# Optimization experiments

Hardware: AMD Instinct MI355X
Metric: run time of the kernel (lower is better)

The kernel has to match this reference:

```python
import jax, jax.numpy as jnp
import numpy as np
from jax import lax

EPS = 1e-5
C, H, W, G = 512, 32, 32, 32


def instance_norm(x):
    # torch InstanceNorm2d: affine=False, biased variance over (H,W)
    mu = x.mean(axis=(2, 3), keepdims=True)
    var = ((x - mu) ** 2).mean(axis=(2, 3), keepdims=True)
    return (x - mu) / jnp.sqrt(var + EPS)


def conv2d(x, w, stride=1, padding=0, groups=1, lhs_dilation=None):
    return lax.conv_general_dilated(
        x, w, (stride, stride), [(padding, padding)] * 2,
        lhs_dilation=lhs_dilation, feature_group_count=groups,
        dimension_numbers=('NCHW', 'OIHW', 'NCHW'))


def leaky_relu(x):
    return jnp.where(x >= 0, x, 0.2 * x)


def unfold(img, k, s):
    # img: (C,H,W) -> (nH*nW, C, k, k); matches torch unfold(1,k,s).unfold(2,k,s)
    c, h, w = img.shape
    nH = (h - k) // s + 1
    nW = (w - k) // s + 1
    rows = []
    for i in range(k):
        cols = [img[:, i:i + s * (nH - 1) + 1:s, j:j + s * (nW - 1) + 1:s] for j in range(k)]
        rows.append(jnp.stack(cols, axis=-1))  # (C,nH,nW,k)
    p = jnp.stack(rows, axis=-2)  # (C,nH,nW,k,k)
    return p.transpose(1, 2, 0, 3, 4).reshape(nH * nW, c, k, k)


def ral(bg, fg, rate=2, ksize=3, scale=10.0):
    # Region Affinity Layer (contextual-attention style), batch = 1
    b, c, h, w = fg.shape
    fh, fw = h // rate, w // rate
    # bilinear downsample by exactly 2 (half-pixel) == 2x2 average pooling
    fg_small = fg.reshape(b, c, fh, rate, fw, rate).mean(axis=(3, 5))
    bk = 2 * rate
    bg_patches = unfold(jnp.pad(bg, ((0, 0), (0, 0), (1, 1), (1, 1)))[0], bk, rate)      # (256,C,4,4)
    fg_patches = unfold(jnp.pad(fg_small, ((0, 0), (0, 0), (1, 1), (1, 1)))[0], ksize, 1)  # (256,C,3,3)
    norm = jnp.sqrt((fg_patches ** 2).sum(axis=(1, 2, 3), keepdims=True))
    fgp_n = fg_patches / jnp.maximum(norm, 1e-4)
    score = conv2d(fg_small, fgp_n, padding=1)        # (1,256,16,16)
    attn = jax.nn.softmax(score * scale, axis=1)
    # conv_transpose2d(attn, bg_patches, stride=rate, padding=1) via lhs dilation
    w_t = jnp.flip(bg_patches, axis=(-2, -1)).transpose(1, 0, 2, 3)  # (C,256,4,4)
    return conv2d(attn, w_t, padding=bk - 2, lhs_dilation=(rate, rate)) / 4.0  # (1,C,32,32)


def forward(x, gus, w_sk3, b_sk3, w_sk5, b_sk5, w_sk7, b_sk7,
            w_fc, b_fc, w_fc0, b_fc0, w_fc1, b_fc1, w_fc2, b_fc2, w_down, w_fuse):
    # ---- SKConv (M=3 branches: k=3/5/7, groups=32) ----
    feas = []
    for wgt, bias, pad in ((w_sk3, b_sk3, 1), (w_sk5, b_sk5, 2), (w_sk7, b_sk7, 3)):
        f = conv2d(x, wgt, padding=pad, groups=G) + bias[None, :, None, None]
        feas.append(jax.nn.relu(instance_norm(f)))
    feas = jnp.stack(feas, axis=1)                # (B,3,C,H,W)
    fea_s = feas.sum(axis=1).mean(axis=(2, 3))    # (B,C) global pool
    fea_z = fea_s @ w_fc.T + b_fc                 # (B,32)
    att = jnp.stack([fea_z @ w_fc0.T + b_fc0,
                     fea_z @ w_fc1.T + b_fc1,
                     fea_z @ w_fc2.T + b_fc2], axis=1)  # (B,3,C)
    att = jax.nn.softmax(att, axis=1)[..., None, None]
    out_32 = (feas * att).sum(axis=1)             # (1,C,32,32)
    out_res = out_32
    out_32 = ral(out_32, out_32)
    b, c, h, w = out_32.shape
    # ---- gaussian-weighted broadcast sum: (P,H,W)x(C,H,W)->(P,C)->raw reshape ----
    gus_out = jnp.einsum('pxy,cxy->pc', gus, out_32[0]).reshape(b, c, h, w)
    # ---- CSA patch correlation ----
    csa2_in = jax.nn.sigmoid(out_32)
    p_fff = unfold(jnp.pad(out_32, ((0, 0), (0, 0), (1, 1), (1, 1)))[0], 3, 1)    # (1024,C,3,3)
    p_f = unfold(jnp.pad(csa2_in, ((0, 0), (0, 0), (1, 1), (1, 1)))[0], 3, 1)     # (1024,C,3,3)
    p_conv = unfold(csa2_in[0], 1, 1)                                             # (1024,C,1,1)
    csa_a = (p_conv * p_f).mean(axis=1)                                           # (1024,3,3)
    csa_a = jax.nn.softmax(csa_a.reshape(h * w, 9), axis=1).reshape(h * w, 1, 3, 3)
    out_csa = (csa_a * p_fff).sum(axis=(-2, -1)).reshape(b, c, h, w)
    # ---- fuse ----
    z = jnp.concatenate([gus_out, out_csa], axis=1)       # (1,1024,32,32)
    z = leaky_relu(instance_norm(conv2d(z, w_down)))
    z = jnp.concatenate([z, out_res], axis=1)             # (1,1024,32,32)
    return leaky_relu(instance_norm(conv2d(z, w_fuse)))   # (1,512,32,32)


def _gaussian_buffer():
    # util.gussin(1.5): gaussian centered at every grid position of a 32x32 map
    v = 1.5
    r = np.arange(32)
    i, k, x, y = np.meshgrid(r, r, r, r, indexing='ij')
    g = np.exp(-((x - i) ** 2 + (y - k) ** 2) / (2 * v * v)) / (2 * np.pi * v * v)
    return jnp.asarray(g.reshape(32 * 32, 32, 32), dtype=jnp.float32)


def setup_inputs():
    key = jax.random.key(0)
    ks = jax.random.split(key, 12)
    s = 0.02
    return {
        'x': jax.random.normal(ks[0], (1, C, H, W), jnp.float32),
        'gus': _gaussian_buffer(),
        'w_sk3': jax.random.normal(ks[1], (C, C // G, 3, 3), jnp.float32) * s,
        'b_sk3': jnp.zeros((C,), jnp.float32),
        'w_sk5': jax.random.normal(ks[2], (C, C // G, 5, 5), jnp.float32) * s,
        'b_sk5': jnp.zeros((C,), jnp.float32),
        'w_sk7': jax.random.normal(ks[3], (C, C // G, 7, 7), jnp.float32) * s,
        'b_sk7': jnp.zeros((C,), jnp.float32),
        'w_fc': jax.random.normal(ks[4], (32, C), jnp.float32) * s,
        'b_fc': jnp.zeros((32,), jnp.float32),
        'w_fc0': jax.random.normal(ks[5], (C, 32), jnp.float32) * s,
        'b_fc0': jnp.zeros((C,), jnp.float32),
        'w_fc1': jax.random.normal(ks[6], (C, 32), jnp.float32) * s,
        'b_fc1': jnp.zeros((C,), jnp.float32),
        'w_fc2': jax.random.normal(ks[7], (C, 32), jnp.float32) * s,
        'b_fc2': jnp.zeros((C,), jnp.float32),
        'w_down': jax.random.normal(ks[8], (512, 1024, 1, 1), jnp.float32) * s,
        'w_fuse': jax.random.normal(ks[9], (512, 1024, 1, 1), jnp.float32) * s,
    }


def reference(x, gus, w_sk3, b_sk3, w_sk5, b_sk5, w_sk7, b_sk7, w_fc, b_fc,
              w_fc0, b_fc0, w_fc1, b_fc1, w_fc2, b_fc2, w_down, w_fuse):
    return forward(x, gus, w_sk3, b_sk3, w_sk5, b_sk5, w_sk7, b_sk7,
                   w_fc, b_fc, w_fc0, b_fc0, w_fc1, b_fc1, w_fc2, b_fc2,
                   w_down, w_fuse)
```

## Files before the change

### kernel.cpp

```cpp
#include <hip/hip_runtime.h>
#include <math.h>

#define EPSN 1e-5f

typedef __attribute__((ext_vector_type(8))) short bf16x8;
typedef __attribute__((ext_vector_type(4))) float f32x4;

__device__ __forceinline__ ushort f2bf(float f) {
  unsigned u = __float_as_uint(f);
  unsigned r = (u + 0x7fff + ((u >> 16) & 1)) >> 16;
  return (ushort)r;
}
__device__ __forceinline__ float bf2f(ushort h) {
  return __uint_as_float(((unsigned)h) << 16);
}

__device__ __forceinline__ void breduce2(float& a, float& b, float* lds) {
#pragma unroll
  for (int o = 32; o > 0; o >>= 1) {
    a += __shfl_down(a, o);
    b += __shfl_down(b, o);
  }
  int lane = threadIdx.x & 63, wid = threadIdx.x >> 6;
  __syncthreads();
  if (lane == 0) { lds[wid] = a; lds[4 + wid] = b; }
  __syncthreads();
  a = lds[0] + lds[1] + lds[2] + lds[3];
  b = lds[4] + lds[5] + lds[6] + lds[7];
}

__device__ __forceinline__ float breduce_sum(float v, float* lds) {
#pragma unroll
  for (int o = 32; o > 0; o >>= 1) v += __shfl_down(v, o);
  int lane = threadIdx.x & 63, wid = threadIdx.x >> 6;
  __syncthreads();
  if (lane == 0) lds[wid] = v;
  __syncthreads();
  return lds[0] + lds[1] + lds[2] + lds[3];
}

__device__ __forceinline__ float breduce_max(float v, float* lds) {
#pragma unroll
  for (int o = 32; o > 0; o >>= 1) v = fmaxf(v, __shfl_down(v, o));
  int lane = threadIdx.x & 63, wid = threadIdx.x >> 6;
  __syncthreads();
  if (lane == 0) lds[wid] = v;
  __syncthreads();
  return fmaxf(fmaxf(lds[0], lds[1]), fmaxf(lds[2], lds[3]));
}

__global__ void pre_kernel(const float* __restrict__ gus,
                           const float* __restrict__ wdown,
                           const float* __restrict__ wfuse,
                           const float* __restrict__ w3,
                           const float* __restrict__ w5,
                           const float* __restrict__ w7,
                           ushort* __restrict__ gus_bf,
                           ushort* __restrict__ wdown_bf,
                           ushort* __restrict__ wfuse_bf,
                           ushort* __restrict__ resd,
                           ushort* __restrict__ Apk_g,
                           ushort* __restrict__ Acomb,
                           float* __restrict__ diagsum) {
  int bid = blockIdx.x, tid = threadIdx.x;
  if (bid < 2048) {
    int i = bid * 1024 + tid * 4;
    if (i < 1048576) {
      float4 v = *(const float4*)&gus[i];
      int m = i >> 10, n = i & 1023;
      int y = n >> 5, x = n & 31;
      int idxb = ((y >> 1) << 4) + (x >> 1);
      int py = y & 1;
      ushort2 e0 = {f2bf(v.x), f2bf(v.z)};
      ushort2 e1 = {f2bf(v.y), f2bf(v.w)};
      *(ushort2*)&gus_bf[(size_t)m * 1024 + (py * 2 + 0) * 256 + idxb] = e0;
      *(ushort2*)&gus_bf[(size_t)m * 1024 + (py * 2 + 1) * 256 + idxb] = e1;
    } else {
      const float* src; ushort* dst; int off;
      if (i < 1572864) { src = wdown; dst = wdown_bf; off = i - 1048576; }
      else { src = wfuse; dst = wfuse_bf; off = i - 1572864; }
      float4 v = *(const float4*)&src[off];
      ushort4 o = {f2bf(v.x), f2bf(v.y), f2bf(v.z), f2bf(v.w)};
      *(ushort4*)&dst[off] = o;
    }
  } else if (bid < 2304) {
    int t8 = (bid - 2048) * 256 + tid;
    uint4 z = {0u, 0u, 0u, 0u};
#pragma unroll
    for (int k = 0; k < 4; ++k) *(uint4*)&resd[(size_t)(t8 + k * 65536) * 8] = z;
  } else if (bid < 5056) {
    int i2 = (bid - 2304) * 256 + tid;
    int g = i2 / 22016;
    int r = i2 - g * 22016;
    int p = r >> 9;
    int r5 = r & 511;
    int quad = r5 >> 7, m16 = (r5 >> 3) & 15, j = r & 7;
    int k = quad * 8 + j, tp = k >> 4, ic = k & 15;
    float val = 0.f;
    if (p < 25) {
      int t = 2 * p + tp;
      if (t < 49) val = w7[(size_t)(g * 16 + m16) * 784 + ic * 49 + t];
    } else if (p < 38) {
      int t = 2 * (p - 25) + tp;
      if (t < 25) val = w5[(size_t)(g * 16 + m16) * 400 + ic * 25 + t];
    } else {
      int t = 2 * (p - 38) + tp;
      if (t < 9) val = w3[(size_t)(g * 16 + m16) * 144 + ic * 9 + t];
    }
    Apk_g[i2] = f2bf(val);
  } else if (bid < 5568) {
    int j = (bid - 5056) * 256 + tid;
    uint4 z = {0u, 0u, 0u, 0u};
    ((uint4*)Acomb)[j] = z;
  } else {
    diagsum[tid] = 0.f;
  }
}

__global__ __launch_bounds__(256) void sk_mfma(const float* __restrict__ x,
                                               const ushort* __restrict__ Apk_g,
                                               ushort* __restrict__ feasRawH) {
  __shared__ ushort xg[10 * 38 * 24];
  int bid = blockIdx.x, tid = threadIdx.x;
  int g = bid >> 3, sl = bid & 7, y0 = sl * 4;
  for (int i = tid; i < 4560; i += 256) ((uint*)xg)[i] = 0u;
  __syncthreads();
  for (int i = tid; i < 5120; i += 256) {
    int lr = i >> 9, ic = (i >> 5) & 15, xc = i & 31;
    int y = y0 + lr - 3;
    if ((unsigned)y < 32u)
      xg[(lr * 38 + xc + 3) * 24 + ic] =
          f2bf(x[(size_t)(g * 16 + ic) * 1024 + y * 32 + xc]);
  }
  __syncthreads();
  int wv = tid >> 6, lane = tid & 63, quad = lane >> 4, m16 = lane & 15;
  int qh = (quad & 1) * 8, tp = quad >> 1;
  const ushort* Ag = Apk_g + (size_t)g * 22016;
  f32x4 acc[2][3] = {};
#pragma unroll
  for (int p = 0; p < 25; ++p) {
    bf16x8 af = *(const bf16x8*)&Ag[(p * 4 + quad) * 128 + m16 * 8];
    int t = 2 * p + tp;
    if (t > 48) t = 48;
    int ky = t / 7, kx = t - ky * 7;
#pragma unroll
    for (int ti = 0; ti < 2; ++ti) {
      int T = wv + ti * 4, tl = T >> 1, x0c = (T & 1) * 16;
      bf16x8 bf = *(const bf16x8*)&xg[((tl + ky) * 38 + x0c + m16 + kx) * 24 + qh];
      acc[ti][2] = __builtin_amdgcn_mfma_f32_16x16x32_bf16(af, bf, acc[ti][2], 0, 0, 0);
    }
  }
#pragma unroll
  for (int p = 0; p < 13; ++p) {
    bf16x8 af = *(const bf16x8*)&Ag[((p + 25) * 4 + quad) * 128 + m16 * 8];
    int t = 2 * p + tp;
    if (t > 24) t = 24;
    int ky = t / 5, kx = t - ky * 5;
#pragma unroll
    for (int ti = 0; ti < 2; ++ti) {
      int T = wv + ti * 4, tl = T >> 1, x0c = (T & 1) * 16;
      bf16x8 bf =
          *(const bf16x8*)&xg[((tl + ky + 1) * 38 + x0c + m16 + kx + 1) * 24 + qh];
      acc[ti][1] = __builtin_amdgcn_mfma_f32_16x16x32_bf16(af, bf, acc[ti][1], 0, 0, 0);
    }
  }
#pragma unroll
  for (int p = 0; p < 5; ++p) {
    bf16x8 af = *(const bf16x8*)&Ag[((p + 38) * 4 + quad) * 128 + m16 * 8];
    int t = 2 * p + tp;
    if (t > 8) t = 8;
    int ky = t / 3, kx = t - ky * 3;
#pragma unroll
    for (int ti = 0; ti < 2; ++ti) {
      int T = wv + ti * 4, tl = T >> 1, x0c = (T & 1) * 16;
      bf16x8 bf =
          *(const bf16x8*)&xg[((tl + ky + 2) * 38 + x0c + m16 + kx + 2) * 24 + qh];
      acc[ti][0] = __builtin_amdgcn_mfma_f32_16x16x32_bf16(af, bf, acc[ti][0], 0, 0, 0);
    }
  }
  int cb = g * 16 + quad * 4;
#pragma unroll
  for (int ti = 0; ti < 2; ++ti) {
    int T = wv + ti * 4, tl = T >> 1, x0c = (T & 1) * 16;
    int pos = (y0 + tl) * 32 + x0c + m16;
#pragma unroll
    for (int br = 0; br < 3; ++br)
#pragma unroll
      for (int r = 0; r < 4; ++r)
        feasRawH[(size_t)(br * 512 + cb + r) * 1024 + pos] = f2bf(acc[ti][br][r]);
  }
}

__global__ __launch_bounds__(256) void sk_norm(const ushort* __restrict__ rawH,
                                               ushort* __restrict__ feasH,
                                               float* __restrict__ bmean) {
  __shared__ float red[8];
  int mc = blockIdx.x, tid = threadIdx.x;
  float v[4];
  {
    ushort4 h = *(const ushort4*)&rawH[(size_t)mc * 1024 + tid * 4];
    v[0] = bf2f(h.x); v[1] = bf2f(h.y); v[2] = bf2f(h.z); v[3] = bf2f(h.w);
  }
  float s = 0.f, ss = 0.f;
#pragma unroll
  for (int r = 0; r < 4; ++r) { s += v[r]; ss += v[r] * v[r]; }
  breduce2(s, ss, red);
  float mean = s * (1.f / 1024.f);
  float var = ss * (1.f / 1024.f) - mean * mean;
  float inv = rsqrtf(var + EPSN);
  float rs = 0.f;
  ushort4 o;
#pragma unroll
  for (int r = 0; r < 4; ++r) {
    float t = (v[r] - mean) * inv;
    t = t > 0.f ? t : 0.f;
    ((ushort*)&o)[r] = f2bf(t);
    rs += t;
  }
  *(ushort4*)&feasH[(size_t)mc * 1024 + tid * 4] = o;
  float tot = breduce_sum(rs, red);
  if (tid == 0) bmean[mc] = tot * (1.f / 1024.f);
}

__global__ __launch_bounds__(256) void blend_fc(
    const ushort* __restrict__ feasH, const float* __restrict__ bmean,
    const float* __restrict__ wfc, const float* __restrict__ bfc,
    const float* __restrict__ w0, const float* __restrict__ b0,
    const float* __restrict__ w1, const float* __restrict__ b1,
    const float* __restrict__ w2, const float* __restrict__ b2,
    float* __restrict__ res, ushort* __restrict__ Zt2,
    ushort* __restrict__ resd) {
  __shared__ float sfea[512];
  __shared__ float zpart[8][32];
  __shared__ float zz[32];
  __shared__ float lv[3][32];
  __shared__ float attb[3][32];
  __shared__ float tile[32][33];
  int tid = threadIdx.x;
  int pb = blockIdx.x * 32, cb = blockIdx.y * 32;
  for (int c = tid; c < 512; c += 256)
    sfea[c] = bmean[c] + bmean[512 + c] + bmean[1024 + c];
  __syncthreads();
  {
    int j = tid & 31, seg = tid >> 5;
    float p = 0.f;
    for (int c = seg * 64; c < seg * 64 + 64; ++c) p += sfea[c] * wfc[j * 512 + c];
    zpart[seg][j] = p;
  }
  __syncthreads();
  if (tid < 32) {
    float d = bfc[tid];
#pragma unroll
    for (int s = 0; s < 8; ++s) d += zpart[s][tid];
    zz[tid] = d;
  }
  __syncthreads();
  if (tid < 96) {
    int m = tid >> 5, cl = tid & 31;
    const float* wm = (m == 0) ? w0 : (m == 1) ? w1 : w2;
    const float* bm = (m == 0) ? b0 : (m == 1) ? b1 : b2;
    float l = bm[cb + cl];
#pragma unroll
    for (int j = 0; j < 32; ++j) l += zz[j] * wm[(cb + cl) * 32 + j];
    lv[m][cl] = l;
  }
  __syncthreads();
  if (tid < 32) {
    float l0 = lv[0][tid], l1 = lv[1][tid], l2 = lv[2][tid];
    float mx = fmaxf(l0, fmaxf(l1, l2));
    float e0 = expf(l0 - mx), e1 = expf(l1 - mx), e2 = expf(l2 - mx);
    float inv = 1.f / (e0 + e1 + e2);
    attb[0][tid] = e0 * inv; attb[1][tid] = e1 * inv; attb[2][tid] = e2 * inv;
  }
  __syncthreads();
  int tx = tid & 31, ty = tid >> 5;
  int pos = pb + tx;
  int yy = pos >> 5, xx = pos & 31;
  int ki0 = (yy + 1) & 1, pi0 = (yy + 1 - ki0) >> 1;
  int kj0 = (xx + 1) & 1, pj0 = (xx + 1 - kj0) >> 1;
#pragma unroll
  for (int r = 0; r < 4; ++r) {
    int cl = ty + r * 8;
    int c = cb + cl;
    float v = bf2f(feasH[(size_t)c * 1024 + pos]) * attb[0][cl] +
              bf2f(feasH[(size_t)(512 + c) * 1024 + pos]) * attb[1][cl] +
              bf2f(feasH[(size_t)(1024 + c) * 1024 + pos]) * attb[2][cl];
    res[c * 1024 + pos] = v;
    tile[cl][tx] = v;
    ushort bv16 = f2bf(v);
#pragma unroll
    for (int ai = 0; ai < 2; ++ai) {
      int ki = ki0 + 2 * ai, pi = pi0 - ai;
      if ((unsigned)pi >= 16u) continue;
#pragma unroll
      for (int aj = 0; aj < 2; ++aj) {
        int kj = kj0 + 2 * aj, pj = pj0 - aj;
        if ((unsigned)pj >= 16u) continue;
        resd[((size_t)(ki * 4 + kj) << 17) + (size_t)c * 256 + pi * 16 + pj] = bv16;
      }
    }
  }
  __syncthreads();
#pragma unroll
  for (int r = 0; r < 4; ++r) {
    int pl = ty + r * 8;
    Zt2[(size_t)(pb + pl) * 1024 + 512 + cb + tx] = f2bf(tile[tx][pl]);
  }
}

__global__ __launch_bounds__(256) void gram_part2(const float* __restrict__ res,
                                                  float* __restrict__ Apart,
                                                  float* __restrict__ diagsum) {
  __shared__ float ch[4][324];
  const int PBT[10] = {0, 0, 0, 0, 1, 1, 1, 2, 2, 3};
  const int QBT[10] = {0, 1, 2, 3, 1, 2, 3, 2, 3, 3};
  int tid = threadIdx.x;
  int pid = blockIdx.x;
  int pb = PBT[pid] * 64, qb = QBT[pid] * 64;
  int kc = blockIdx.z;
  int tx = tid & 15, ty = tid >> 4;
  for (int i = tid; i < 4 * 324; i += 256) ((float*)ch)[i] = 0.f;
  int pi = (pb + ty * 4) >> 4, pj = (pb + ty * 4) & 15;
  int qi = (qb + tx * 4) >> 4, qj = (qb + tx * 4) & 15;
  int lane = tid & 63, wv = tid >> 6;
  int sr = lane >> 2, sc = (lane & 3) * 4;
  float acc[4][4] = {};
  for (int c0 = kc * 16; c0 < kc * 16 + 16; c0 += 4) {
    __syncthreads();
    {
      const float* src = res + (size_t)(c0 + wv) * 1024 + (2 * sr) * 32 + 2 * sc;
      float4 r0a = *(const float4*)src;
      float4 r0b = *(const float4*)(src + 4);
      float4 r1a = *(const float4*)(src + 32);
      float4 r1b = *(const float4*)(src + 36);
      float* dst = &ch[wv][(sr + 1) * 18 + sc + 1];
      dst[0] = 0.25f * (r0a.x + r0a.y + r1a.x + r1a.y);
      dst[1] = 0.25f * (r0a.z + r0a.w + r1a.z + r1a.w);
      dst[2] = 0.25f * (r0b.x + r0b.y + r1b.x + r1b.y);
      dst[3] = 0.25f * (r0b.z + r0b.w + r1b.z + r1b.w);
    }
    __syncthreads();
#pragma unroll
    for (int cc = 0; cc < 4; ++cc) {
      float ps[3][6], qs[3][6];
#pragma unroll
      for (int u = 0; u < 3; ++u) {
        const float* pr = &ch[cc][(pi + u) * 18 + pj];
        const float* qr = &ch[cc][(qi + u) * 18 + qj];
#pragma unroll
        for (int t = 0; t < 6; ++t) { ps[u][t] = pr[t]; qs[u][t] = qr[t]; }
      }
#pragma unroll
      for (int u = 0; u < 3; ++u)
#pragma unroll
        for (int v = 0; v < 3; ++v)
#pragma unroll
          for (int i = 0; i < 4; ++i)
#pragma unroll
            for (int j = 0; j < 4; ++j)
              acc[i][j] += ps[u][v + i] * qs[u][v + j];
    }
  }
#pragma unroll
  for (int i = 0; i < 4; ++i) {
    float4 o4 = {acc[i][0], acc[i][1], acc[i][2], acc[i][3]};
    *(float4*)&Apart[(size_t)kc * 65536 + (pb + ty * 4 + i) * 256 + qb + tx * 4] = o4;
  }
  if (pb != qb) {
#pragma unroll
    for (int j = 0; j < 4; ++j) {
      float4 o4 = {acc[0][j], acc[1][j], acc[2][j], acc[3][j]};
      *(float4*)&Apart[(size_t)kc * 65536 + (qb + tx * 4 + j) * 256 + pb + ty * 4] = o4;
    }
  } else if (tx == ty) {
#pragma unroll
    for (int i = 0; i < 4; ++i) atomicAdd(&diagsum[pb + tx * 4 + i], acc[i][i]);
  }
}

__global__ __launch_bounds__(256) void attn_soft4(const float* __restrict__ Apart,
                                                  const float* __restrict__ diagsum,
                                                  ushort* __restrict__ Acomb) {
  __shared__ float red[8];
  int q = blockIdx.x, t = threadIdx.x;
  float d = diagsum[t];
  float s = 0.f;
#pragma unroll
  for (int k = 0; k < 32; ++k) s += Apart[(size_t)k * 65536 + q * 256 + t];
  float invn = 10.f / fmaxf(sqrtf(fmaxf(d, 0.f)), 1e-4f);
  float v = s * invn;
  float mx = breduce_max(v, red);
  float e = expf(v - mx);
  float sm = breduce_sum(e, red);
  ushort val = f2bf(e / sm);
  int qi = q >> 4, qj = q & 15;
#pragma unroll
  for (int ki = 0; ki < 4; ++ki) {
    int y = 2 * qi + ki - 1;
    if ((unsigned)y >= 32u) continue;
#pragma unroll
    for (int kj = 0; kj < 4; ++kj) {
      int x = 2 * qj + kj - 1;
      if ((unsigned)x >= 32u) continue;
      int cls = (y & 1) * 2 + (x & 1);
      int idx = ((y >> 1) << 4) + (x >> 1);
      int seg = ((ki >> 1) << 1) + (kj >> 1);
      Acomb[(size_t)(cls * 256 + idx) * 1024 + seg * 256 + t] = val;
    }
  }
}

__global__ __launch_bounds__(256) void tconv2(const ushort* __restrict__ Acomb,
                                              const ushort* __restrict__ resd,
                                              float* __restrict__ orlt,
                                              float* __restrict__ sigt,
                                              ushort* __restrict__ orlT) {
  __shared__ float tl[64][33];
  int tid = threadIdx.x;
  int wv = tid >> 6, lane = tid & 63, quad = lane >> 4, m16 = lane & 15;
  int nb = blockIdx.x * 32;
  int mb = blockIdx.y * 64;
  int cls = blockIdx.y >> 2;
  int py = cls >> 1, px = cls & 1;
  int row0 = mb + wv * 16 + m16;
  const ushort* Ap = Acomb + (size_t)row0 * 1024 + quad * 8;
  f32x4 ac0 = {0.f, 0.f, 0.f, 0.f}, ac1 = ac0;
#pragma unroll
  for (int sg = 0; sg < 4; ++sg) {
    int ki = 2 * (sg >> 1) + 1 - py;
    int kj = 2 * (sg & 1) + 1 - px;
    const ushort* Bp =
        resd + ((size_t)(ki * 4 + kj) << 17) + (size_t)(nb + m16) * 256 + quad * 8;
    const ushort* As = Ap + sg * 256;
#pragma unroll 4
    for (int k0 = 0; k0 < 256; k0 += 32) {
      bf16x8 af = *(const bf16x8*)(As + k0);
      bf16x8 b0 = *(const bf16x8*)(Bp + k0);
      bf16x8 b1 = *(const bf16x8*)(Bp + 16 * 256 + k0);
      ac0 = __builtin_amdgcn_mfma_f32_16x16x32_bf16(af, b0, ac0, 0, 0, 0);
      ac1 = __builtin_amdgcn_mfma_f32_16x16x32_bf16(af, b1, ac1, 0, 0, 0);
    }
  }
  int rloc0 = wv * 16 + quad * 4;
  f32x4 accs[2] = {ac0, ac1};
#pragma unroll
  for (int nt = 0; nt < 2; ++nt) {
    int c = nb + nt * 16 + m16;
#pragma unroll
    for (int r = 0; r < 4; ++r) {
      int rl = rloc0 + r;
      int idx = (mb + rl) & 255;
      int y = ((idx >> 4) << 1) + py;
      int x = ((idx & 15) << 1) + px;
      int n = y * 32 + x;
      float v = accs[nt][r] * 0.25f;
      orlt[n * 512 + c] = v;
      sigt[n * 512 + c] = 1.f / (1.f + expf(-v));
      tl[rl][nt * 16 + m16] = v;
    }
  }
  __syncthreads();
  int r_l = tid & 63;
#pragma unroll
  for (int k = 0; k < 8; ++k) {
    int c_l = (tid >> 6) + k * 4;
    orlT[(size_t)(nb + c_l) * 1024 + mb + r_l] = f2bf(tl[r_l][c_l]);
  }
}

__global__ __launch_bounds__(256) void gus_csa(
    const ushort* __restrict__ gus_bf, const ushort* __restrict__ orlT,
    const float* __restrict__ sigt, const float* __restrict__ orlt,
    ushort* __restrict__ Zt) {
  __shared__ float red9[4][9];
  __shared__ float a9s[9];
  int tid = threadIdx.x;
  if (blockIdx.x < 128) {
    const int K = 1024;
    int wv = tid >> 6, lane = tid & 63;
    int quad = lane >> 4, m16 = lane & 15;
    int nb = (blockIdx.x & 7) * 64, mb = (blockIdx.x >> 3) * 64;
    const ushort* Ap = gus_bf + (size_t)(mb + wv * 16 + m16) * K + quad * 8;
    const ushort* Bp = orlT + (size_t)(nb + m16) * K + quad * 8;
    f32x4 ac0 = {0.f, 0.f, 0.f, 0.f}, ac1 = ac0, ac2 = ac0, ac3 = ac0;
#pragma unroll 4
    for (int k0 = 0; k0 < K; k0 += 32) {
      bf16x8 af = *(const bf16x8*)(Ap + k0);
      bf16x8 b0 = *(const bf16x8*)(Bp + k0);
      bf16x8 b1 = *(const bf16x8*)(Bp + (size_t)16 * K + k0);
      bf16x8 b2 = *(const bf16x8*)(Bp + (size_t)32 * K + k0);
      bf16x8 b3 = *(const bf16x8*)(Bp + (size_t)48 * K + k0);
      ac0 = __builtin_amdgcn_mfma_f32_16x16x32_bf16(af, b0, ac0, 0, 0, 0);
      ac1 = __builtin_amdgcn_mfma_f32_16x16x32_bf16(af, b1, ac1, 0, 0, 0);
      ac2 = __builtin_amdgcn_mfma_f32_16x16x32_bf16(af, b2, ac2, 0, 0, 0);
      ac3 = __builtin_amdgcn_mfma_f32_16x16x32_bf16(af, b3, ac3, 0, 0, 0);
    }
    int row = mb + wv * 16 + quad * 4;
    f32x4 accs[4] = {ac0, ac1, ac2, ac3};
#pragma unroll
    for (int nt = 0; nt < 4; ++nt) {
      int c = nb + nt * 16 + m16;
#pragma unroll
      for (int r = 0; r < 4; ++r) {
        int p = row + r;
        int pos = ((p & 1) << 9) + c;
        int kk = p >> 1;
        Zt[(size_t)pos * 1024 + kk] = f2bf(accs[nt][r]);
      }
    }
    return;
  }
  int n = blockIdx.x - 128;
  int ny = n >> 5, nx = n & 31;
  int c2 = tid * 2;
  int lane = tid & 63, wid = tid >> 6;
  float2 ctr = *(const float2*)&sigt[n * 512 + c2];
  float part[9];
#pragma unroll
  for (int u = 0; u < 3; ++u) {
    int yy = ny + u - 1;
#pragma unroll
    for (int v = 0; v < 3; ++v) {
      int xx = nx + v - 1;
      float2 nb2 = {0.f, 0.f};
      if ((unsigned)yy < 32u && (unsigned)xx < 32u)
        nb2 = *(const float2*)&sigt[(yy * 32 + xx) * 512 + c2];
      part[u * 3 + v] = ctr.x * nb2.x + ctr.y * nb2.y;
    }
  }
#pragma unroll
  for (int t = 0; t < 9; ++t)
#pragma unroll
    for (int o = 32; o > 0; o >>= 1) part[t] += __shfl_down(part[t], o);
  if (lane == 0)
#pragma unroll
    for (int t = 0; t < 9; ++t) red9[wid][t] = part[t];
  __syncthreads();
  if (tid == 0) {
    float a[9];
#pragma unroll
    for (int t = 0; t < 9; ++t)
      a[t] = (red9[0][t] + red9[1][t] + red9[2][t] + red9[3][t]) * (1.f / 512.f);
    float mx = a[0];
#pragma unroll
    for (int t = 1; t < 9; ++t) mx = fmaxf(mx, a[t]);
    float sum = 0.f;
#pragma unroll
    for (int t = 0; t < 9; ++t) { a[t] = expf(a[t] - mx); sum += a[t]; }
    float inv = 1.f / sum;
#pragma unroll
    for (int t = 0; t < 9; ++t) a9s[t] = a[t] * inv;
  }
  __syncthreads();
  float2 acc = {0.f, 0.f};
#pragma unroll
  for (int u = 0; u < 3; ++u) {
    int yy = ny + u - 1;
#pragma unroll
    for (int v = 0; v < 3; ++v) {
      int xx = nx + v - 1;
      if ((unsigned)yy < 32u && (unsigned)xx < 32u) {
        float w = a9s[u * 3 + v];
        float2 ov = *(const float2*)&orlt[(yy * 32 + xx) * 512 + c2];
        acc.x += w * ov.x;
        acc.y += w * ov.y;
      }
    }
  }
  int kk = 512 + (n >> 1);
  int pos0 = ((n & 1) << 9) + c2;
  Zt[(size_t)pos0 * 1024 + kk] = f2bf(acc.x);
  Zt[(size_t)(pos0 + 1) * 1024 + kk] = f2bf(acc.y);
}

__global__ __launch_bounds__(256) void mfma_gemm_ks(const ushort* __restrict__ A,
                                                    const ushort* __restrict__ Bt,
                                                    float* __restrict__ Cp,
                                                    int N) {
  const int KF = 1024;
  int tid = threadIdx.x;
  int wv = tid >> 6, lane = tid & 63;
  int quad = lane >> 4, m16 = lane & 15;
  int nb = blockIdx.x * 64, mb = blockIdx.y * 64;
  int kh = blockIdx.z;
  const ushort* Ap = A + (size_t)(mb + wv * 16 + m16) * KF + kh * 512 + quad * 8;
  const ushort* Bp = Bt + (size_t)(nb + m16) * KF + kh * 512 + quad * 8;
  f32x4 ac0 = {0.f, 0.f, 0.f, 0.f}, ac1 = ac0, ac2 = ac0, ac3 = ac0;
#pragma unroll 4
  for (int k0 = 0; k0 < 512; k0 += 32) {
    bf16x8 af = *(const bf16x8*)(Ap + k0);
    bf16x8 b0 = *(const bf16x8*)(Bp + k0);
    bf16x8 b1 = *(const bf16x8*)(Bp + (size_t)16 * KF + k0);
    bf16x8 b2 = *(const bf16x8*)(Bp + (size_t)32 * KF + k0);
    bf16x8 b3 = *(const bf16x8*)(Bp + (size_t)48 * KF + k0);
    ac0 = __builtin_amdgcn_mfma_f32_16x16x32_bf16(af, b0, ac0, 0, 0, 0);
    ac1 = __builtin_amdgcn_mfma_f32_16x16x32_bf16(af, b1, ac1, 0, 0, 0);
    ac2 = __builtin_amdgcn_mfma_f32_16x16x32_bf16(af, b2, ac2, 0, 0, 0);
    ac3 = __builtin_amdgcn_mfma_f32_16x16x32_bf16(af, b3, ac3, 0, 0, 0);
  }
  int row = mb + wv * 16 + quad * 4;
  float* C = Cp + (size_t)kh * 524288;
  f32x4 accs[4] = {ac0, ac1, ac2, ac3};
#pragma unroll
  for (int nt = 0; nt < 4; ++nt)
#pragma unroll
    for (int r = 0; r < 4; ++r)
      C[(size_t)(row + r) * N + nb + nt * 16 + m16] = accs[nt][r];
}

__global__ __launch_bounds__(256) void norm_down2(const float* __restrict__ ra,
                                                  ushort* __restrict__ Zt2) {
  __shared__ float red[8];
  int c = blockIdx.x, tid = threadIdx.x;
  float v[4];
  float s = 0.f, ss = 0.f;
#pragma unroll
  for (int r = 0; r < 4; ++r) {
    int i = c * 1024 + tid + r * 256;
    v[r] = ra[i] + ra[524288 + i];
    s += v[r];
    ss += v[r] * v[r];
  }
  breduce2(s, ss, red);
  float mean = s * (1.f / 1024.f);
  float var = ss * (1.f / 1024.f) - mean * mean;
  float inv = rsqrtf(var + EPSN);
#pragma unroll
  for (int r = 0; r < 4; ++r) {
    float t = (v[r] - mean) * inv;
    t = t >= 0.f ? t : 0.2f * t;
    Zt2[(size_t)(tid + r * 256) * 1024 + c] = f2bf(t);
  }
}

__global__ __launch_bounds__(256) void norm_leaky2(const float* __restrict__ ra,
                                                   float* __restrict__ out) {
  __shared__ float red[8];
  int c = blockIdx.x, tid = threadIdx.x;
  float v[4];
  float s = 0.f, ss = 0.f;
#pragma unroll
  for (int r = 0; r < 4; ++r) {
    int i = c * 1024 + tid + r * 256;
    v[r] = ra[i] + ra[524288 + i];
    s += v[r];
    ss += v[r] * v[r];
  }
  breduce2(s, ss, red);
  float mean = s * (1.f / 1024.f);
  float var = ss * (1.f / 1024.f) - mean * mean;
  float inv = rsqrtf(var + EPSN);
#pragma unroll
  for (int r = 0; r < 4; ++r) {
    float t = (v[r] - mean) * inv;
    out[c * 1024 + tid + r * 256] = t >= 0.f ? t : 0.2f * t;
  }
}

extern "C" void kernel_launch(void* const* d_in, const int* in_sizes, int n_in,
                              void* d_out, int out_size, void* d_ws, size_t ws_size,
                              hipStream_t stream) {
  const float* x = (const float*)d_in[0];
  const float* gus = (const float*)d_in[1];
  const float* w3 = (const float*)d_in[2];
  const float* w5 = (const float*)d_in[4];
  const float* w7 = (const float*)d_in[6];
  const float* wfc = (const float*)d_in[8];
  const float* bfc = (const float*)d_in[9];
  const float* w0 = (const float*)d_in[10];
  const float* b0 = (const float*)d_in[11];
  const float* w1 = (const float*)d_in[12];
  const float* b1 = (const float*)d_in[13];
  const float* w2 = (const float*)d_in[14];
  const float* b2 = (const float*)d_in[15];
  const float* wdown = (const float*)d_in[16];
  const float* wfuse = (const float*)d_in[17];

  float* ws = (float*)d_ws;
  ushort* feasH = (ushort*)ws;
  float* rawP = ws + 786432;
  ushort* Acomb = (ushort*)rawP;
  float* bmean = ws + 1835008;
  float* res = bmean + 1536;
  float* Zt2f = res + 524288;
  ushort* Zt2 = (ushort*)Zt2f;
  float* T = Zt2f + 524288;
  ushort* feasRawH = (ushort*)T;
  float* Apart = T;
  ushort* Zt = (ushort*)T;
  float* orlt = T + 2097152;
  float* sigt = orlt + 524288;
  ushort* orlT = (ushort*)(sigt + 524288);
  ushort* gus_bf = (ushort*)(sigt + 819200);
  ushort* wdown_bf = (ushort*)(sigt + 1343488);
  ushort* wfuse_bf = (ushort*)(sigt + 1605632);
  ushort* resd = (ushort*)(sigt + 1867776);
  ushort* Apk_g = (ushort*)(sigt + 2916352);
  float* diagsum = sigt + 3268608;

  pre_kernel<<<5569, 256, 0, stream>>>(gus, wdown, wfuse, w3, w5, w7, gus_bf,
                                       wdown_bf, wfuse_bf, resd, Apk_g, Acomb,
                                       diagsum);
  sk_mfma<<<256, 256, 0, stream>>>(x, Apk_g, feasRawH);
  sk_norm<<<1536, 256, 0, stream>>>(feasRawH, feasH, bmean);
  blend_fc<<<dim3(32, 16), 256, 0, stream>>>(feasH, bmean, wfc, bfc, w0, b0, w1,
                                             b1, w2, b2, res, Zt2, resd);
  gram_part2<<<dim3(10, 1, 32), 256, 0, stream>>>(res, Apart, diagsum);
  attn_soft4<<<256, 256, 0, stream>>>(Apart, diagsum, Acomb);
  tconv2<<<dim3(16, 16), 256, 0, stream>>>(Acomb, resd, orlt, sigt, orlT);
  gus_csa<<<1152, 256, 0, stream>>>(gus_bf, orlT, sigt, orlt, Zt);
  mfma_gemm_ks<<<dim3(16, 8, 2), 256, 0, stream>>>(wdown_bf, Zt, rawP, 1024);
  norm_down2<<<512, 256, 0, stream>>>(rawP, Zt2);
  mfma_gemm_ks<<<dim3(16, 8, 2), 256, 0, stream>>>(wfuse_bf, Zt2, rawP, 1024);
  norm_leaky2<<<512, 256, 0, stream>>>(rawP, (float*)d_out);
}
```

Baseline: 217.5 us.

## Fuse all post-prep kernels into one persistent kernel with grid barriers

Replaces eleven sequential kernel launches with a single 256-block persistent kernel. Each former kernel becomes a stage, and stages are separated by atomic-counter grid barriers whose counters are zeroed in the prep kernel. Stages that used to launch more blocks now loop with grid-stride. The aim is to remove launch gaps and inter-kernel drain time. The cost is barrier spin overhead, lower parallelism for the stages that had more blocks, and a deadlock risk if the 256 blocks are not all co-resident.

```diff
diff --git a/kernel.cpp b/kernel.cpp
--- a/kernel.cpp
+++ b/kernel.cpp
@@ -47,6 +47,19 @@
   if (lane == 0) lds[wid] = v;
   __syncthreads();
   return fmaxf(fmaxf(lds[0], lds[1]), fmaxf(lds[2], lds[3]));
+}
+
+__device__ __forceinline__ void gridbar(unsigned* bar) {
+  __syncthreads();
+  if (threadIdx.x == 0) {
+    __threadfence();
+    unsigned old = atomicAdd(bar, 1u);
+    if (old != 255u) {
+      while (atomicAdd(bar, 0u) < 256u) __builtin_amdgcn_s_sleep(16);
+    }
+    __threadfence();
+  }
+  __syncthreads();
 }
 
 __global__ void pre_kernel(const float* __restrict__ gus,
@@ -61,7 +74,8 @@
                            ushort* __restrict__ resd,
                            ushort* __restrict__ Apk_g,
                            ushort* __restrict__ Acomb,
-                           float* __restrict__ diagsum) {
+                           float* __restrict__ diagsum,
+                           unsigned* __restrict__ bar) {
   int bid = blockIdx.x, tid = threadIdx.x;
   if (bid < 2048) {
     int i = bid * 1024 + tid * 4;
@@ -114,546 +128,579 @@
     ((uint4*)Acomb)[j] = z;
   } else {
     diagsum[tid] = 0.f;
-  }
-}
-
-__global__ __launch_bounds__(256) void sk_mfma(const float* __restrict__ x,
-                                               const ushort* __restrict__ Apk_g,
-                                               ushort* __restrict__ feasRawH) {
-  __shared__ ushort xg[10 * 38 * 24];
-  int bid = blockIdx.x, tid = threadIdx.x;
-  int g = bid >> 3, sl = bid & 7, y0 = sl * 4;
-  for (int i = tid; i < 4560; i += 256) ((uint*)xg)[i] = 0u;
-  __syncthreads();
-  for (int i = tid; i < 5120; i += 256) {
-    int lr = i >> 9, ic = (i >> 5) & 15, xc = i & 31;
-    int y = y0 + lr - 3;
-    if ((unsigned)y < 32u)
-      xg[(lr * 38 + xc + 3) * 24 + ic] =
-          f2bf(x[(size_t)(g * 16 + ic) * 1024 + y * 32 + xc]);
-  }
-  __syncthreads();
-  int wv = tid >> 6, lane = tid & 63, quad = lane >> 4, m16 = lane & 15;
-  int qh = (quad & 1) * 8, tp = quad >> 1;
-  const ushort* Ag = Apk_g + (size_t)g * 22016;
-  f32x4 acc[2][3] = {};
-#pragma unroll
-  for (int p = 0; p < 25; ++p) {
-    bf16x8 af = *(const bf16x8*)&Ag[(p * 4 + quad) * 128 + m16 * 8];
-    int t = 2 * p + tp;
-    if (t > 48) t = 48;
-    int ky = t / 7, kx = t - ky * 7;
-#pragma unroll
-    for (int ti = 0; ti < 2; ++ti) {
-      int T = wv + ti * 4, tl = T >> 1, x0c = (T & 1) * 16;
-      bf16x8 bf = *(const bf16x8*)&xg[((tl + ky) * 38 + x0c + m16 + kx) * 24 + qh];
-      acc[ti][2] = __builtin_amdgcn_mfma_f32_16x16x32_bf16(af, bf, acc[ti][2], 0, 0, 0);
-    }
-  }
-#pragma unroll
-  for (int p = 0; p < 13; ++p) {
-    bf16x8 af = *(const bf16x8*)&Ag[((p + 25) * 4 + quad) * 128 + m16 * 8];
-    int t = 2 * p + tp;
-    if (t > 24) t = 24;
-    int ky = t / 5, kx = t - ky * 5;
-#pragma unroll
-    for (int ti = 0; ti < 2; ++ti) {
-      int T = wv + ti * 4, tl = T >> 1, x0c = (T & 1) * 16;
-      bf16x8 bf =
-          *(const bf16x8*)&xg[((tl + ky + 1) * 38 + x0c + m16 + kx + 1) * 24 + qh];
-      acc[ti][1] = __builtin_amdgcn_mfma_f32_16x16x32_bf16(af, bf, acc[ti][1], 0, 0, 0);
-    }
-  }
-#pragma unroll
-  for (int p = 0; p < 5; ++p) {
-    bf16x8 af = *(const bf16x8*)&Ag[((p + 38) * 4 + quad) * 128 + m16 * 8];
-    int t = 2 * p + tp;
-    if (t > 8) t = 8;
-    int ky = t / 3, kx = t - ky * 3;
-#pragma unroll
-    for (int ti = 0; ti < 2; ++ti) {
-      int T = wv + ti * 4, tl = T >> 1, x0c = (T & 1) * 16;
-      bf16x8 bf =
-          *(const bf16x8*)&xg[((tl + ky + 2) * 38 + x0c + m16 + kx + 2) * 24 + qh];
-      acc[ti][0] = __builtin_amdgcn_mfma_f32_16x16x32_bf16(af, bf, acc[ti][0], 0, 0, 0);
-    }
-  }
-  int cb = g * 16 + quad * 4;
-#pragma unroll
-  for (int ti = 0; ti < 2; ++ti) {
-    int T = wv + ti * 4, tl = T >> 1, x0c = (T & 1) * 16;
-    int pos = (y0 + tl) * 32 + x0c + m16;
-#pragma unroll
-    for (int br = 0; br < 3; ++br)
-#pragma unroll
-      for (int r = 0; r < 4; ++r)
-        feasRawH[(size_t)(br * 512 + cb + r) * 1024 + pos] = f2bf(acc[ti][br][r]);
-  }
-}
-
-__global__ __launch_bounds__(256) void sk_norm(const ushort* __restrict__ rawH,
-                                               ushort* __restrict__ feasH,
-                                               float* __restrict__ bmean) {
-  __shared__ float red[8];
-  int mc = blockIdx.x, tid = threadIdx.x;
-  float v[4];
-  {
-    ushort4 h = *(const ushort4*)&rawH[(size_t)mc * 1024 + tid * 4];
-    v[0] = bf2f(h.x); v[1] = bf2f(h.y); v[2] = bf2f(h.z); v[3] = bf2f(h.w);
-  }
-  float s = 0.f, ss = 0.f;
-#pragma unroll
-  for (int r = 0; r < 4; ++r) { s += v[r]; ss += v[r] * v[r]; }
-  breduce2(s, ss, red);
-  float mean = s * (1.f / 1024.f);
-  float var = ss * (1.f / 1024.f) - mean * mean;
-  float inv = rsqrtf(var + EPSN);
-  float rs = 0.f;
-  ushort4 o;
-#pragma unroll
-  for (int r = 0; r < 4; ++r) {
-    float t = (v[r] - mean) * inv;
-    t = t > 0.f ? t : 0.f;
-    ((ushort*)&o)[r] = f2bf(t);
-    rs += t;
-  }
-  *(ushort4*)&feasH[(size_t)mc * 1024 + tid * 4] = o;
-  float tot = breduce_sum(rs, red);
-  if (tid == 0) bmean[mc] = tot * (1.f / 1024.f);
-}
-
-__global__ __launch_bounds__(256) void blend_fc(
-    const ushort* __restrict__ feasH, const float* __restrict__ bmean,
+    if (tid < 16) bar[tid] = 0u;
+  }
+}
+
+__global__ __launch_bounds__(256) void mega(
+    const float* __restrict__ x,
+    const ushort* __restrict__ Apk_g,
+    ushort* feasH, float* bmean,
     const float* __restrict__ wfc, const float* __restrict__ bfc,
     const float* __restrict__ w0, const float* __restrict__ b0,
     const float* __restrict__ w1, const float* __restrict__ b1,
     const float* __restrict__ w2, const float* __restrict__ b2,
-    float* __restrict__ res, ushort* __restrict__ Zt2,
-    ushort* __restrict__ resd) {
-  __shared__ float sfea[512];
-  __shared__ float zpart[8][32];
-  __shared__ float zz[32];
-  __shared__ float lv[3][32];
-  __shared__ float attb[3][32];
-  __shared__ float tile[32][33];
-  int tid = threadIdx.x;
-  int pb = blockIdx.x * 32, cb = blockIdx.y * 32;
-  for (int c = tid; c < 512; c += 256)
-    sfea[c] = bmean[c] + bmean[512 + c] + bmean[1024 + c];
-  __syncthreads();
-  {
-    int j = tid & 31, seg = tid >> 5;
-    float p = 0.f;
-    for (int c = seg * 64; c < seg * 64 + 64; ++c) p += sfea[c] * wfc[j * 512 + c];
-    zpart[seg][j] = p;
-  }
-  __syncthreads();
-  if (tid < 32) {
-    float d = bfc[tid];
-#pragma unroll
-    for (int s = 0; s < 8; ++s) d += zpart[s][tid];
-    zz[tid] = d;
-  }
-  __syncthreads();
-  if (tid < 96) {
-    int m = tid >> 5, cl = tid & 31;
-    const float* wm = (m == 0) ? w0 : (m == 1) ? w1 : w2;
-    const float* bm = (m == 0) ? b0 : (m == 1) ? b1 : b2;
-    float l = bm[cb + cl];
-#pragma unroll
-    for (int j = 0; j < 32; ++j) l += zz[j] * wm[(cb + cl) * 32 + j];
-    lv[m][cl] = l;
-  }
-  __syncthreads();
-  if (tid < 32) {
-    float l0 = lv[0][tid], l1 = lv[1][tid], l2 = lv[2][tid];
-    float mx = fmaxf(l0, fmaxf(l1, l2));
-    float e0 = expf(l0 - mx), e1 = expf(l1 - mx), e2 = expf(l2 - mx);
-    float inv = 1.f / (e0 + e1 + e2);
-    attb[0][tid] = e0 * inv; attb[1][tid] = e1 * inv; attb[2][tid] = e2 * inv;
-  }
-  __syncthreads();
-  int tx = tid & 31, ty = tid >> 5;
-  int pos = pb + tx;
-  int yy = pos >> 5, xx = pos & 31;
-  int ki0 = (yy + 1) & 1, pi0 = (yy + 1 - ki0) >> 1;
-  int kj0 = (xx + 1) & 1, pj0 = (xx + 1 - kj0) >> 1;
-#pragma unroll
-  for (int r = 0; r < 4; ++r) {
-    int cl = ty + r * 8;
-    int c = cb + cl;
-    float v = bf2f(feasH[(size_t)c * 1024 + pos]) * attb[0][cl] +
-              bf2f(feasH[(size_t)(512 + c) * 1024 + pos]) * attb[1][cl] +
-              bf2f(feasH[(size_t)(1024 + c) * 1024 + pos]) * attb[2][cl];
-    res[c * 1024 + pos] = v;
-    tile[cl][tx] = v;
-    ushort bv16 = f2bf(v);
-#pragma unroll
-    for (int ai = 0; ai < 2; ++ai) {
-      int ki = ki0 + 2 * ai, pi = pi0 - ai;
-      if ((unsigned)pi >= 16u) continue;
-#pragma unroll
-      for (int aj = 0; aj < 2; ++aj) {
-        int kj = kj0 + 2 * aj, pj = pj0 - aj;
-        if ((unsigned)pj >= 16u) continue;
-        resd[((size_t)(ki * 4 + kj) << 17) + (size_t)c * 256 + pi * 16 + pj] = bv16;
-      }
-    }
-  }
-  __syncthreads();
-#pragma unroll
-  for (int r = 0; r < 4; ++r) {
-    int pl = ty + r * 8;
-    Zt2[(size_t)(pb + pl) * 1024 + 512 + cb + tx] = f2bf(tile[tx][pl]);
-  }
-}
-
-__global__ __launch_bounds__(256) void gram_part2(const float* __restrict__ res,
-                                                  float* __restrict__ Apart,
-                                                  float* __restrict__ diagsum) {
-  __shared__ float ch[4][324];
-  const int PBT[10] = {0, 0, 0, 0, 1, 1, 1, 2, 2, 3};
-  const int QBT[10] = {0, 1, 2, 3, 1, 2, 3, 2, 3, 3};
-  int tid = threadIdx.x;
-  int pid = blockIdx.x;
-  int pb = PBT[pid] * 64, qb = QBT[pid] * 64;
-  int kc = blockIdx.z;
-  int tx = tid & 15, ty = tid >> 4;
-  for (int i = tid; i < 4 * 324; i += 256) ((float*)ch)[i] = 0.f;
-  int pi = (pb + ty * 4) >> 4, pj = (pb + ty * 4) & 15;
-  int qi = (qb + tx * 4) >> 4, qj = (qb + tx * 4) & 15;
-  int lane = tid & 63, wv = tid >> 6;
-  int sr = lane >> 2, sc = (lane & 3) * 4;
-  float acc[4][4] = {};
-  for (int c0 = kc * 16; c0 < kc * 16 + 16; c0 += 4) {
-    __syncthreads();
-    {
-      const float* src = res + (size_t)(c0 + wv) * 1024 + (2 * sr) * 32 + 2 * sc;
-      float4 r0a = *(const float4*)src;
-      float4 r0b = *(const float4*)(src + 4);
-      float4 r1a = *(const float4*)(src + 32);
-      float4 r1b = *(const float4*)(src + 36);
-      float* dst = &ch[wv][(sr + 1) * 18 + sc + 1];
-      dst[0] = 0.25f * (r0a.x + r0a.y + r1a.x + r1a.y);
-      dst[1] = 0.25f * (r0a.z + r0a.w + r1a.z + r1a.w);
-      dst[2] = 0.25f * (r0b.x + r0b.y + r1b.x + r1b.y);
-      dst[3] = 0.25f * (r0b.z + r0b.w + r1b.z + r1b.w);
-    }
-    __syncthreads();
-#pragma unroll
-    for (int cc = 0; cc < 4; ++cc) {
-      float ps[3][6], qs[3][6];
-#pragma unroll
-      for (int u = 0; u < 3; ++u) {
-        const float* pr = &ch[cc][(pi + u) * 18 + pj];
-        const float* qr = &ch[cc][(qi + u) * 18 + qj];
-#pragma unroll
-        for (int t = 0; t < 6; ++t) { ps[u][t] = pr[t]; qs[u][t] = qr[t]; }
-      }
-#pragma unroll
-      for (int u = 0; u < 3; ++u)
-#pragma unroll
-        for (int v = 0; v < 3; ++v)
-#pragma unroll
-          for (int i = 0; i < 4; ++i)
-#pragma unroll
-            for (int j = 0; j < 4; ++j)
-              acc[i][j] += ps[u][v + i] * qs[u][v + j];
-    }
-  }
-#pragma unroll
-  for (int i = 0; i < 4; ++i) {
-    float4 o4 = {acc[i][0], acc[i][1], acc[i][2], acc[i][3]};
-    *(float4*)&Apart[(size_t)kc * 65536 + (pb + ty * 4 + i) * 256 + qb + tx * 4] = o4;
-  }
-  if (pb != qb) {
-#pragma unroll
-    for (int j = 0; j < 4; ++j) {
-      float4 o4 = {acc[0][j], acc[1][j], acc[2][j], acc[3][j]};
-      *(float4*)&Apart[(size_t)kc * 65536 + (qb + tx * 4 + j) * 256 + pb + ty * 4] = o4;
-    }
-  } else if (tx == ty) {
-#pragma unroll
-    for (int i = 0; i < 4; ++i) atomicAdd(&diagsum[pb + tx * 4 + i], acc[i][i]);
-  }
-}
-
-__global__ __launch_bounds__(256) void attn_soft4(const float* __restrict__ Apart,
-                                                  const float* __restrict__ diagsum,
-                                                  ushort* __restrict__ Acomb) {
+    float* res, ushort* Zt2, ushort* resd,
+    float* Tbase,
+    float* rawP,
+    float* diagsum,
+    float* orlt, float* sigt, ushort* orlT,
+    const ushort* __restrict__ gus_bf,
+    const ushort* __restrict__ wdown_bf,
+    const ushort* __restrict__ wfuse_bf,
+    float* out, unsigned* bar) {
+  int bid = blockIdx.x, tid = threadIdx.x;
+  ushort* feasRawH = (ushort*)Tbase;
+  float* Apart = Tbase;
+  ushort* Zt = (ushort*)Tbase;
+  ushort* Acomb = (ushort*)rawP;
+
+  __shared__ union SM {
+    ushort xg[9120];
+    struct {
+      float sfea[512], zpart[8][32], zz[32], lv[3][32], attb[3][32], tile[32][33];
+    } bl;
+    float ch[4][324];
+    float tl[64][33];
+  } sm;
   __shared__ float red[8];
-  int q = blockIdx.x, t = threadIdx.x;
-  float d = diagsum[t];
-  float s = 0.f;
-#pragma unroll
-  for (int k = 0; k < 32; ++k) s += Apart[(size_t)k * 65536 + q * 256 + t];
-  float invn = 10.f / fmaxf(sqrtf(fmaxf(d, 0.f)), 1e-4f);
-  float v = s * invn;
-  float mx = breduce_max(v, red);
-  float e = expf(v - mx);
-  float sm = breduce_sum(e, red);
-  ushort val = f2bf(e / sm);
-  int qi = q >> 4, qj = q & 15;
-#pragma unroll
-  for (int ki = 0; ki < 4; ++ki) {
-    int y = 2 * qi + ki - 1;
-    if ((unsigned)y >= 32u) continue;
-#pragma unroll
-    for (int kj = 0; kj < 4; ++kj) {
-      int x = 2 * qj + kj - 1;
-      if ((unsigned)x >= 32u) continue;
-      int cls = (y & 1) * 2 + (x & 1);
-      int idx = ((y >> 1) << 4) + (x >> 1);
-      int seg = ((ki >> 1) << 1) + (kj >> 1);
-      Acomb[(size_t)(cls * 256 + idx) * 1024 + seg * 256 + t] = val;
-    }
-  }
-}
-
-__global__ __launch_bounds__(256) void tconv2(const ushort* __restrict__ Acomb,
-                                              const ushort* __restrict__ resd,
-                                              float* __restrict__ orlt,
-                                              float* __restrict__ sigt,
-                                              ushort* __restrict__ orlT) {
-  __shared__ float tl[64][33];
-  int tid = threadIdx.x;
-  int wv = tid >> 6, lane = tid & 63, quad = lane >> 4, m16 = lane & 15;
-  int nb = blockIdx.x * 32;
-  int mb = blockIdx.y * 64;
-  int cls = blockIdx.y >> 2;
-  int py = cls >> 1, px = cls & 1;
-  int row0 = mb + wv * 16 + m16;
-  const ushort* Ap = Acomb + (size_t)row0 * 1024 + quad * 8;
-  f32x4 ac0 = {0.f, 0.f, 0.f, 0.f}, ac1 = ac0;
-#pragma unroll
-  for (int sg = 0; sg < 4; ++sg) {
-    int ki = 2 * (sg >> 1) + 1 - py;
-    int kj = 2 * (sg & 1) + 1 - px;
-    const ushort* Bp =
-        resd + ((size_t)(ki * 4 + kj) << 17) + (size_t)(nb + m16) * 256 + quad * 8;
-    const ushort* As = Ap + sg * 256;
-#pragma unroll 4
-    for (int k0 = 0; k0 < 256; k0 += 32) {
-      bf16x8 af = *(const bf16x8*)(As + k0);
-      bf16x8 b0 = *(const bf16x8*)(Bp + k0);
-      bf16x8 b1 = *(const bf16x8*)(Bp + 16 * 256 + k0);
-      ac0 = __builtin_amdgcn_mfma_f32_16x16x32_bf16(af, b0, ac0, 0, 0, 0);
-      ac1 = __builtin_amdgcn_mfma_f32_16x16x32_bf16(af, b1, ac1, 0, 0, 0);
-    }
-  }
-  int rloc0 = wv * 16 + quad * 4;
-  f32x4 accs[2] = {ac0, ac1};
-#pragma unroll
-  for (int nt = 0; nt < 2; ++nt) {
-    int c = nb + nt * 16 + m16;
-#pragma unroll
-    for (int r = 0; r < 4; ++r) {
-      int rl = rloc0 + r;
-      int idx = (mb + rl) & 255;
-      int y = ((idx >> 4) << 1) + py;
-      int x = ((idx & 15) << 1) + px;
-      int n = y * 32 + x;
-      float v = accs[nt][r] * 0.25f;
-      orlt[n * 512 + c] = v;
-      sigt[n * 512 + c] = 1.f / (1.f + expf(-v));
-      tl[rl][nt * 16 + m16] = v;
-    }
-  }
-  __syncthreads();
-  int r_l = tid & 63;
-#pragma unroll
-  for (int k = 0; k < 8; ++k) {
-    int c_l = (tid >> 6) + k * 4;
-    orlT[(size_t)(nb + c_l) * 1024 + mb + r_l] = f2bf(tl[r_l][c_l]);
-  }
-}
-
-__global__ __launch_bounds__(256) void gus_csa(
-    const ushort* __restrict__ gus_bf, const ushort* __restrict__ orlT,
-    const float* __restrict__ sigt, const float* __restrict__ orlt,
-    ushort* __restrict__ Zt) {
   __shared__ float red9[4][9];
   __shared__ float a9s[9];
-  int tid = threadIdx.x;
-  if (blockIdx.x < 128) {
-    const int K = 1024;
+
+  {
+    int g = bid >> 3, sl = bid & 7, y0 = sl * 4;
+    for (int i = tid; i < 4560; i += 256) ((uint*)sm.xg)[i] = 0u;
+    __syncthreads();
+    for (int i = tid; i < 5120; i += 256) {
+      int lr = i >> 9, ic = (i >> 5) & 15, xc = i & 31;
+      int y = y0 + lr - 3;
+      if ((unsigned)y < 32u)
+        sm.xg[(lr * 38 + xc + 3) * 24 + ic] =
+            f2bf(x[(size_t)(g * 16 + ic) * 1024 + y * 32 + xc]);
+    }
+    __syncthreads();
+    int wv = tid >> 6, lane = tid & 63, quad = lane >> 4, m16 = lane & 15;
+    int qh = (quad & 1) * 8, tp = quad >> 1;
+    const ushort* Ag = Apk_g + (size_t)g * 22016;
+    f32x4 acc[2][3] = {};
+#pragma unroll
+    for (int p = 0; p < 25; ++p) {
+      bf16x8 af = *(const bf16x8*)&Ag[(p * 4 + quad) * 128 + m16 * 8];
+      int t = 2 * p + tp;
+      if (t > 48) t = 48;
+      int ky = t / 7, kx = t - ky * 7;
+#pragma unroll
+      for (int ti = 0; ti < 2; ++ti) {
+        int T = wv + ti * 4, tl = T >> 1, x0c = (T & 1) * 16;
+        bf16x8 bf = *(const bf16x8*)&sm.xg[((tl + ky) * 38 + x0c + m16 + kx) * 24 + qh];
+        acc[ti][2] = __builtin_amdgcn_mfma_f32_16x16x32_bf16(af, bf, acc[ti][2], 0, 0, 0);
+      }
+    }
+#pragma unroll
+    for (int p = 0; p < 13; ++p) {
+      bf16x8 af = *(const bf16x8*)&Ag[((p + 25) * 4 + quad) * 128 + m16 * 8];
+      int t = 2 * p + tp;
+      if (t > 24) t = 24;
+      int ky = t / 5, kx = t - ky * 5;
+#pragma unroll
+      for (int ti = 0; ti < 2; ++ti) {
+        int T = wv + ti * 4, tl = T >> 1, x0c = (T & 1) * 16;
+        bf16x8 bf =
+            *(const bf16x8*)&sm.xg[((tl + ky + 1) * 38 + x0c + m16 + kx + 1) * 24 + qh];
+        acc[ti][1] = __builtin_amdgcn_mfma_f32_16x16x32_bf16(af, bf, acc[ti][1], 0, 0, 0);
+      }
+    }
+#pragma unroll
+    for (int p = 0; p < 5; ++p) {
+      bf16x8 af = *(const bf16x8*)&Ag[((p + 38) * 4 + quad) * 128 + m16 * 8];
+      int t = 2 * p + tp;
+      if (t > 8) t = 8;
+      int ky = t / 3, kx = t - ky * 3;
+#pragma unroll
+      for (int ti = 0; ti < 2; ++ti) {
+        int T = wv + ti * 4, tl = T >> 1, x0c = (T & 1) * 16;
+        bf16x8 bf =
+            *(const bf16x8*)&sm.xg[((tl + ky + 2) * 38 + x0c + m16 + kx + 2) * 24 + qh];
+        acc[ti][0] = __builtin_amdgcn_mfma_f32_16x16x32_bf16(af, bf, acc[ti][0], 0, 0, 0);
+      }
+    }
+    int cb = g * 16 + quad * 4;
+#pragma unroll
+    for (int ti = 0; ti < 2; ++ti) {
+      int T = wv + ti * 4, tl = T >> 1, x0c = (T & 1) * 16;
+      int pos = (y0 + tl) * 32 + x0c + m16;
+#pragma unroll
+      for (int br = 0; br < 3; ++br)
+#pragma unroll
+        for (int r = 0; r < 4; ++r)
+          feasRawH[(size_t)(br * 512 + cb + r) * 1024 + pos] = f2bf(acc[ti][br][r]);
+    }
+  }
+  gridbar(&bar[0]);
+
+  for (int vb = bid; vb < 1536; vb += 256) {
+    int mc = vb;
+    float v[4];
+    {
+      ushort4 h = *(const ushort4*)&feasRawH[(size_t)mc * 1024 + tid * 4];
+      v[0] = bf2f(h.x); v[1] = bf2f(h.y); v[2] = bf2f(h.z); v[3] = bf2f(h.w);
+    }
+    float s = 0.f, ss = 0.f;
+#pragma unroll
+    for (int r = 0; r < 4; ++r) { s += v[r]; ss += v[r] * v[r]; }
+    breduce2(s, ss, red);
+    float mean = s * (1.f / 1024.f);
+    float var = ss * (1.f / 1024.f) - mean * mean;
+    float inv = rsqrtf(var + EPSN);
+    float rs = 0.f;
+    ushort4 o;
+#pragma unroll
+    for (int r = 0; r < 4; ++r) {
+      float t = (v[r] - mean) * inv;
+      t = t > 0.f ? t : 0.f;
+      ((ushort*)&o)[r] = f2bf(t);
+      rs += t;
+    }
+    *(ushort4*)&feasH[(size_t)mc * 1024 + tid * 4] = o;
+    float tot = breduce_sum(rs, red);
+    if (tid == 0) bmean[mc] = tot * (1.f / 1024.f);
+  }
+  gridbar(&bar[1]);
+
+  for (int vb = bid; vb < 512; vb += 256) {
+    int pb = (vb & 31) * 32, cb = (vb >> 5) * 32;
+    for (int c = tid; c < 512; c += 256)
+      sm.bl.sfea[c] = bmean[c] + bmean[512 + c] + bmean[1024 + c];
+    __syncthreads();
+    {
+      int j = tid & 31, seg = tid >> 5;
+      float p = 0.f;
+      for (int c = seg * 64; c < seg * 64 + 64; ++c)
+        p += sm.bl.sfea[c] * wfc[j * 512 + c];
+      sm.bl.zpart[seg][j] = p;
+    }
+    __syncthreads();
+    if (tid < 32) {
+      float d = bfc[tid];
+#pragma unroll
+      for (int s = 0; s < 8; ++s) d += sm.bl.zpart[s][tid];
+      sm.bl.zz[tid] = d;
+    }
+    __syncthreads();
+    if (tid < 96) {
+      int m = tid >> 5, cl = tid & 31;
+      const float* wm = (m == 0) ? w0 : (m == 1) ? w1 : w2;
+      const float* bm = (m == 0) ? b0 : (m == 1) ? b1 : b2;
+      float l = bm[cb + cl];
+#pragma unroll
+      for (int j = 0; j < 32; ++j) l += sm.bl.zz[j] * wm[(cb + cl) * 32 + j];
+      sm.bl.lv[m][cl] = l;
+    }
+    __syncthreads();
+    if (tid < 32) {
+      float l0 = sm.bl.lv[0][tid], l1 = sm.bl.lv[1][tid], l2 = sm.bl.lv[2][tid];
+      float mx = fmaxf(l0, fmaxf(l1, l2));
+      float e0 = expf(l0 - mx), e1 = expf(l1 - mx), e2 = expf(l2 - mx);
+      float inv = 1.f / (e0 + e1 + e2);
+      sm.bl.attb[0][tid] = e0 * inv;
+      sm.bl.attb[1][tid] = e1 * inv;
+      sm.bl.attb[2][tid] = e2 * inv;
+    }
+    __syncthreads();
+    int tx = tid & 31, ty = tid >> 5;
+    int pos = pb + tx;
+    int yy = pos >> 5, xx = pos & 31;
+    int ki0 = (yy + 1) & 1, pi0 = (yy + 1 - ki0) >> 1;
+    int kj0 = (xx + 1) & 1, pj0 = (xx + 1 - kj0) >> 1;
+#pragma unroll
+    for (int r = 0; r < 4; ++r) {
+      int cl = ty + r * 8;
+      int c = cb + cl;
+      float v = bf2f(feasH[(size_t)c * 1024 + pos]) * sm.bl.attb[0][cl] +
+                bf2f(feasH[(size_t)(512 + c) * 1024 + pos]) * sm.bl.attb[1][cl] +
+                bf2f(feasH[(size_t)(1024 + c) * 1024 + pos]) * sm.bl.attb[2][cl];
+      res[c * 1024 + pos] = v;
+      sm.bl.tile[cl][tx] = v;
+      ushort bv16 = f2bf(v);
+#pragma unroll
+      for (int ai = 0; ai < 2; ++ai) {
+        int ki = ki0 + 2 * ai, pi = pi0 - ai;
+        if ((unsigned)pi >= 16u) continue;
+#pragma unroll
+        for (int aj = 0; aj < 2; ++aj) {
+          int kj = kj0 + 2 * aj, pj = pj0 - aj;
+          if ((unsigned)pj >= 16u) continue;
+          resd[((size_t)(ki * 4 + kj) << 17) + (size_t)c * 256 + pi * 16 + pj] = bv16;
+        }
+      }
+    }
+    __syncthreads();
+#pragma unroll
+    for (int r = 0; r < 4; ++r) {
+      int pl = ty + r * 8;
+      Zt2[(size_t)(pb + pl) * 1024 + 512 + cb + tx] = f2bf(sm.bl.tile[tx][pl]);
+    }
+    __syncthreads();
+  }
+  gridbar(&bar[2]);
+
+  for (int vb = bid; vb < 320; vb += 256) {
+    const int PBT[10] = {0, 0, 0, 0, 1, 1, 1, 2, 2, 3};
+    const int QBT[10] = {0, 1, 2, 3, 1, 2, 3, 2, 3, 3};
+    int pid = vb % 10, kc = vb / 10;
+    int pb = PBT[pid] * 64, qb = QBT[pid] * 64;
+    int tx = tid & 15, ty = tid >> 4;
+    for (int i = tid; i < 4 * 324; i += 256) ((float*)sm.ch)[i] = 0.f;
+    int pi = (pb + ty * 4) >> 4, pj = (pb + ty * 4) & 15;
+    int qi = (qb + tx * 4) >> 4, qj = (qb + tx * 4) & 15;
+    int lane = tid & 63, wv = tid >> 6;
+    int sr = lane >> 2, sc = (lane & 3) * 4;
+    float acc[4][4] = {};
+    for (int c0 = kc * 16; c0 < kc * 16 + 16; c0 += 4) {
+      __syncthreads();
+      {
+        const float* src = res + (size_t)(c0 + wv) * 1024 + (2 * sr) * 32 + 2 * sc;
+        float4 r0a = *(const float4*)src;
+        float4 r0b = *(const float4*)(src + 4);
+        float4 r1a = *(const float4*)(src + 32);
+        float4 r1b = *(const float4*)(src + 36);
+        float* dst = &sm.ch[wv][(sr + 1) * 18 + sc + 1];
+        dst[0] = 0.25f * (r0a.x + r0a.y + r1a.x + r1a.y);
+        dst[1] = 0.25f * (r0a.z + r0a.w + r1a.z + r1a.w);
+        dst[2] = 0.25f * (r0b.x + r0b.y + r1b.x + r1b.y);
+        dst[3] = 0.25f * (r0b.z + r0b.w + r1b.z + r1b.w);
+      }
+      __syncthreads();
+#pragma unroll
+      for (int cc = 0; cc < 4; ++cc) {
+        float ps[3][6], qs[3][6];
+#pragma unroll
+        for (int u = 0; u < 3; ++u) {
+          const float* pr = &sm.ch[cc][(pi + u) * 18 + pj];
+          const float* qr = &sm.ch[cc][(qi + u) * 18 + qj];
+#pragma unroll
+          for (int t = 0; t < 6; ++t) { ps[u][t] = pr[t]; qs[u][t] = qr[t]; }
+        }
+#pragma unroll
+        for (int u = 0; u < 3; ++u)
+#pragma unroll
+          for (int v = 0; v < 3; ++v)
+#pragma unroll
+            for (int i = 0; i < 4; ++i)
+#pragma unroll
+              for (int j = 0; j < 4; ++j)
+                acc[i][j] += ps[u][v + i] * qs[u][v + j];
+      }
+    }
+#pragma unroll
+    for (int i = 0; i < 4; ++i) {
+      float4 o4 = {acc[i][0], acc[i][1], acc[i][2], acc[i][3]};
+      *(float4*)&Apart[(size_t)kc * 65536 + (pb + ty * 4 + i) * 256 + qb + tx * 4] = o4;
+    }
+    if (pb != qb) {
+#pragma unroll
+      for (int j = 0; j < 4; ++j) {
+        float4 o4 = {acc[0][j], acc[1][j], acc[2][j], acc[3][j]};
+        *(float4*)&Apart[(size_t)kc * 65536 + (qb + tx * 4 + j) * 256 + pb + ty * 4] = o4;
+      }
+    } else if (tx == ty) {
+#pragma unroll
+      for (int i = 0; i < 4; ++i) atomicAdd(&diagsum[pb + tx * 4 + i], acc[i][i]);
+    }
+    __syncthreads();
+  }
+  gridbar(&bar[3]);
+
+  {
+    int q = bid, t = tid;
+    float d = diagsum[t];
+    float s = 0.f;
+#pragma unroll
+    for (int k = 0; k < 32; ++k) s += Apart[(size_t)k * 65536 + q * 256 + t];
+    float invn = 10.f / fmaxf(sqrtf(fmaxf(d, 0.f)), 1e-4f);
+    float v = s * invn;
+    float mx = breduce_max(v, red);
+    float e = expf(v - mx);
+    float smv = breduce_sum(e, red);
+    ushort val = f2bf(e / smv);
+    int qi = q >> 4, qj = q & 15;
+#pragma unroll
+    for (int ki = 0; ki < 4; ++ki) {
+      int y = 2 * qi + ki - 1;
+      if ((unsigned)y >= 32u) continue;
+#pragma unroll
+      for (int kj = 0; kj < 4; ++kj) {
+        int x2 = 2 * qj + kj - 1;
+        if ((unsigned)x2 >= 32u) continue;
+        int cls = (y & 1) * 2 + (x2 & 1);
+        int idx = ((y >> 1) << 4) + (x2 >> 1);
+        int seg = ((ki >> 1) << 1) + (kj >> 1);
+        Acomb[(size_t)(cls * 256 + idx) * 1024 + seg * 256 + t] = val;
+      }
+    }
+  }
+  gridbar(&bar[4]);
+
+  {
+    int wv = tid >> 6, lane = tid & 63, quad = lane >> 4, m16 = lane & 15;
+    int nb = (bid & 15) * 32;
+    int mb = (bid >> 4) * 64;
+    int cls = bid >> 6;
+    int py = cls >> 1, px = cls & 1;
+    int row0 = mb + wv * 16 + m16;
+    const ushort* Ap = Acomb + (size_t)row0 * 1024 + quad * 8;
+    f32x4 ac0 = {0.f, 0.f, 0.f, 0.f}, ac1 = ac0;
+#pragma unroll
+    for (int sg = 0; sg < 4; ++sg) {
+      int ki = 2 * (sg >> 1) + 1 - py;
+      int kj = 2 * (sg & 1) + 1 - px;
+      const ushort* Bp =
+          resd + ((size_t)(ki * 4 + kj) << 17) + (size_t)(nb + m16) * 256 + quad * 8;
+      const ushort* As = Ap + sg * 256;
+#pragma unroll 4
+      for (int k0 = 0; k0 < 256; k0 += 32) {
+        bf16x8 af = *(const bf16x8*)(As + k0);
+        bf16x8 b0 = *(const bf16x8*)(Bp + k0);
+        bf16x8 b1 = *(const bf16x8*)(Bp + 16 * 256 + k0);
+        ac0 = __builtin_amdgcn_mfma_f32_16x16x32_bf16(af, b0, ac0, 0, 0, 0);
+        ac1 = __builtin_amdgcn_mfma_f32_16x16x32_bf16(af, b1, ac1, 0, 0, 0);
+      }
+    }
+    int rloc0 = wv * 16 + quad * 4;
+    f32x4 accs[2] = {ac0, ac1};
+#pragma unroll
+    for (int nt = 0; nt < 2; ++nt) {
+      int c = nb + nt * 16 + m16;
+#pragma unroll
+      for (int r = 0; r < 4; ++r) {
+        int rl = rloc0 + r;
+        int idx = (mb + rl) & 255;
+        int y = ((idx >> 4) << 1) + py;
+        int x2 = ((idx & 15) << 1) + px;
+        int n = y * 32 + x2;
+        float v = accs[nt][r] * 0.25f;
+        orlt[n * 512 + c] = v;
+        sigt[n * 512 + c] = 1.f / (1.f + expf(-v));
+        sm.tl[rl][nt * 16 + m16] = v;
+      }
+    }
+    __syncthreads();
+    int r_l = tid & 63;
+#pragma unroll
+    for (int k = 0; k < 8; ++k) {
+      int c_l = (tid >> 6) + k * 4;
+      orlT[(size_t)(nb + c_l) * 1024 + mb + r_l] = f2bf(sm.tl[r_l][c_l]);
+    }
+  }
+  gridbar(&bar[5]);
+
+  for (int vb = bid; vb < 1152; vb += 256) {
+    if (vb < 128) {
+      const int K = 1024;
+      int wv = tid >> 6, lane = tid & 63;
+      int quad = lane >> 4, m16 = lane & 15;
+      int nb = (vb & 7) * 64, mb = (vb >> 3) * 64;
+      const ushort* Ap = gus_bf + (size_t)(mb + wv * 16 + m16) * K + quad * 8;
+      const ushort* Bp = orlT + (size_t)(nb + m16) * K + quad * 8;
+      f32x4 ac0 = {0.f, 0.f, 0.f, 0.f}, ac1 = ac0, ac2 = ac0, ac3 = ac0;
+#pragma unroll 4
+      for (int k0 = 0; k0 < K; k0 += 32) {
+        bf16x8 af = *(const bf16x8*)(Ap + k0);
+        bf16x8 b0 = *(const bf16x8*)(Bp + k0);
+        bf16x8 b1 = *(const bf16x8*)(Bp + (size_t)16 * K + k0);
+        bf16x8 b2 = *(const bf16x8*)(Bp + (size_t)32 * K + k0);
+        bf16x8 b3 = *(const bf16x8*)(Bp + (size_t)48 * K + k0);
+        ac0 = __builtin_amdgcn_mfma_f32_16x16x32_bf16(af, b0, ac0, 0, 0, 0);
+        ac1 = __builtin_amdgcn_mfma_f32_16x16x32_bf16(af, b1, ac1, 0, 0, 0);
+        ac2 = __builtin_amdgcn_mfma_f32_16x16x32_bf16(af, b2, ac2, 0, 0, 0);
+        ac3 = __builtin_amdgcn_mfma_f32_16x16x32_bf16(af, b3, ac3, 0, 0, 0);
+      }
+      int row = mb + wv * 16 + quad * 4;
+      f32x4 accs[4] = {ac0, ac1, ac2, ac3};
+#pragma unroll
+      for (int nt = 0; nt < 4; ++nt) {
+        int c = nb + nt * 16 + m16;
+#pragma unroll
+        for (int r = 0; r < 4; ++r) {
+          int p = row + r;
+          int pos = ((p & 1) << 9) + c;
+          int kk = p >> 1;
+          Zt[(size_t)pos * 1024 + kk] = f2bf(accs[nt][r]);
+        }
+      }
+    } else {
+      int n = vb - 128;
+      int ny = n >> 5, nx = n & 31;
+      int c2 = tid * 2;
+      int lane = tid & 63, wid = tid >> 6;
+      float2 ctr = *(const float2*)&sigt[n * 512 + c2];
+      float part[9];
+#pragma unroll
+      for (int u = 0; u < 3; ++u) {
+        int yy = ny + u - 1;
+#pragma unroll
+        for (int v = 0; v < 3; ++v) {
+          int xx = nx + v - 1;
+          float2 nb2 = {0.f, 0.f};
+          if ((unsigned)yy < 32u && (unsigned)xx < 32u)
+            nb2 = *(const float2*)&sigt[(yy * 32 + xx) * 512 + c2];
+          part[u * 3 + v] = ctr.x * nb2.x + ctr.y * nb2.y;
+        }
+      }
+#pragma unroll
+      for (int t = 0; t < 9; ++t)
+#pragma unroll
+        for (int o = 32; o > 0; o >>= 1) part[t] += __shfl_down(part[t], o);
+      __syncthreads();
+      if (lane == 0)
+#pragma unroll
+        for (int t = 0; t < 9; ++t) red9[wid][t] = part[t];
+      __syncthreads();
+      if (tid == 0) {
+        float a[9];
+#pragma unroll
+        for (int t = 0; t < 9; ++t)
+          a[t] = (red9[0][t] + red9[1][t] + red9[2][t] + red9[3][t]) * (1.f / 512.f);
+        float mx = a[0];
+#pragma unroll
+        for (int t = 1; t < 9; ++t) mx = fmaxf(mx, a[t]);
+        float sum = 0.f;
+#pragma unroll
+        for (int t = 0; t < 9; ++t) { a[t] = expf(a[t] - mx); sum += a[t]; }
+        float inv = 1.f / sum;
+#pragma unroll
+        for (int t = 0; t < 9; ++t) a9s[t] = a[t] * inv;
+      }
+      __syncthreads();
+      float2 acc = {0.f, 0.f};
+#pragma unroll
+      for (int u = 0; u < 3; ++u) {
+        int yy = ny + u - 1;
+#pragma unroll
+        for (int v = 0; v < 3; ++v) {
+          int xx = nx + v - 1;
+          if ((unsigned)yy < 32u && (unsigned)xx < 32u) {
+            float w = a9s[u * 3 + v];
+            float2 ov = *(const float2*)&orlt[(yy * 32 + xx) * 512 + c2];
+            acc.x += w * ov.x;
+            acc.y += w * ov.y;
+          }
+        }
+      }
+      int kk = 512 + (n >> 1);
+      int pos0 = ((n & 1) << 9) + c2;
+      Zt[(size_t)pos0 * 1024 + kk] = f2bf(acc.x);
+      Zt[(size_t)(pos0 + 1) * 1024 + kk] = f2bf(acc.y);
+    }
+  }
+  gridbar(&bar[6]);
+
+  {
+    const int KF = 1024;
     int wv = tid >> 6, lane = tid & 63;
     int quad = lane >> 4, m16 = lane & 15;
-    int nb = (blockIdx.x & 7) * 64, mb = (blockIdx.x >> 3) * 64;
-    const ushort* Ap = gus_bf + (size_t)(mb + wv * 16 + m16) * K + quad * 8;
-    const ushort* Bp = orlT + (size_t)(nb + m16) * K + quad * 8;
+    int nb = (bid & 15) * 64, mb = ((bid >> 4) & 7) * 64, kh = bid >> 7;
+    const ushort* Ap = wdown_bf + (size_t)(mb + wv * 16 + m16) * KF + kh * 512 + quad * 8;
+    const ushort* Bp = Zt + (size_t)(nb + m16) * KF + kh * 512 + quad * 8;
     f32x4 ac0 = {0.f, 0.f, 0.f, 0.f}, ac1 = ac0, ac2 = ac0, ac3 = ac0;
 #pragma unroll 4
-    for (int k0 = 0; k0 < K; k0 += 32) {
+    for (int k0 = 0; k0 < 512; k0 += 32) {
       bf16x8 af = *(const bf16x8*)(Ap + k0);
       bf16x8 b0 = *(const bf16x8*)(Bp + k0);
-      bf16x8 b1 = *(const bf16x8*)(Bp + (size_t)16 * K + k0);
-      bf16x8 b2 = *(const bf16x8*)(Bp + (size_t)32 * K + k0);
-      bf16x8 b3 = *(const bf16x8*)(Bp + (size_t)48 * K + k0);
+      bf16x8 b1 = *(const bf16x8*)(Bp + (size_t)16 * KF + k0);
+      bf16x8 b2 = *(const bf16x8*)(Bp + (size_t)32 * KF + k0);
+      bf16x8 b3 = *(const bf16x8*)(Bp + (size_t)48 * KF + k0);
       ac0 = __builtin_amdgcn_mfma_f32_16x16x32_bf16(af, b0, ac0, 0, 0, 0);
       ac1 = __builtin_amdgcn_mfma_f32_16x16x32_bf16(af, b1, ac1, 0, 0, 0);
       ac2 = __builtin_amdgcn_mfma_f32_16x16x32_bf16(af, b2, ac2, 0, 0, 0);
       ac3 = __builtin_amdgcn_mfma_f32_16x16x32_bf16(af, b3, ac3, 0, 0, 0);
     }
     int row = mb + wv * 16 + quad * 4;
+    float* C = rawP + (size_t)kh * 524288;
     f32x4 accs[4] = {ac0, ac1, ac2, ac3};
 #pragma unroll
-    for (int nt = 0; nt < 4; ++nt) {
-      int c = nb + nt * 16 + m16;
-#pragma unroll
-      for (int r = 0; r < 4; ++r) {
-        int p = row + r;
-        int pos = ((p & 1) << 9) + c;
-        int kk = p >> 1;
-        Zt[(size_t)pos * 1024 + kk] = f2bf(accs[nt][r]);
-      }
-    }
-    return;
-  }
-  int n = blockIdx.x - 128;
-  int ny = n >> 5, nx = n & 31;
-  int c2 = tid * 2;
-  int lane = tid & 63, wid = tid >> 6;
-  float2 ctr = *(const float2*)&sigt[n * 512 + c2];
-  float part[9];
-#pragma unroll
-  for (int u = 0; u < 3; ++u) {
-    int yy = ny + u - 1;
-#pragma unroll
-    for (int v = 0; v < 3; ++v) {
-      int xx = nx + v - 1;
-      float2 nb2 = {0.f, 0.f};
-      if ((unsigned)yy < 32u && (unsigned)xx < 32u)
-        nb2 = *(const float2*)&sigt[(yy * 32 + xx) * 512 + c2];
-      part[u * 3 + v] = ctr.x * nb2.x + ctr.y * nb2.y;
-    }
-  }
-#pragma unroll
-  for (int t = 0; t < 9; ++t)
-#pragma unroll
-    for (int o = 32; o > 0; o >>= 1) part[t] += __shfl_down(part[t], o);
-  if (lane == 0)
-#pragma unroll
-    for (int t = 0; t < 9; ++t) red9[wid][t] = part[t];
-  __syncthreads();
-  if (tid == 0) {
-    float a[9];
-#pragma unroll
-    for (int t = 0; t < 9; ++t)
-      a[t] = (red9[0][t] + red9[1][t] + red9[2][t] + red9[3][t]) * (1.f / 512.f);
-    float mx = a[0];
-#pragma unroll
-    for (int t = 1; t < 9; ++t) mx = fmaxf(mx, a[t]);
-    float sum = 0.f;
-#pragma unroll
-    for (int t = 0; t < 9; ++t) { a[t] = expf(a[t] - mx); sum += a[t]; }
-    float inv = 1.f / sum;
-#pragma unroll
-    for (int t = 0; t < 9; ++t) a9s[t] = a[t] * inv;
-  }
-  __syncthreads();
-  float2 acc = {0.f, 0.f};
-#pragma unroll
-  for (int u = 0; u < 3; ++u) {
-    int yy = ny + u - 1;
-#pragma unroll
-    for (int v = 0; v < 3; ++v) {
-      int xx = nx + v - 1;
-      if ((unsigned)yy < 32u && (unsigned)xx < 32u) {
-        float w = a9s[u * 3 + v];
-        float2 ov = *(const float2*)&orlt[(yy * 32 + xx) * 512 + c2];
-        acc.x += w * ov.x;
-        acc.y += w * ov.y;
-      }
-    }
-  }
-  int kk = 512 + (n >> 1);
-  int pos0 = ((n & 1) << 9) + c2;
-  Zt[(size_t)pos0 * 1024 + kk] = f2bf(acc.x);
-  Zt[(size_t)(pos0 + 1) * 1024 + kk] = f2bf(acc.y);
-}
-
-__global__ __launch_bounds__(256) void mfma_gemm_ks(const ushort* __restrict__ A,
-                                                    const ushort* __restrict__ Bt,
-                                                    float* __restrict__ Cp,
-                                                    int N) {
-  const int KF = 1024;
-  int tid = threadIdx.x;
-  int wv = tid >> 6, lane = tid & 63;
-  int quad = lane >> 4, m16 = lane & 15;
-  int nb = blockIdx.x * 64, mb = blockIdx.y * 64;
-  int kh = blockIdx.z;
-  const ushort* Ap = A + (size_t)(mb + wv * 16 + m16) * KF + kh * 512 + quad * 8;
-  const ushort* Bp = Bt + (size_t)(nb + m16) * KF + kh * 512 + quad * 8;
-  f32x4 ac0 = {0.f, 0.f, 0.f, 0.f}, ac1 = ac0, ac2 = ac0, ac3 = ac0;
+    for (int nt = 0; nt < 4; ++nt)
+#pragma unroll
+      for (int r = 0; r < 4; ++r)
+        C[(size_t)(row + r) * 1024 + nb + nt * 16 + m16] = accs[nt][r];
+  }
+  gridbar(&bar[7]);
+
+  for (int vb = bid; vb < 512; vb += 256) {
+    int c = vb;
+    float v[4];
+    float s = 0.f, ss = 0.f;
+#pragma unroll
+    for (int r = 0; r < 4; ++r) {
+      int i = c * 1024 + tid + r * 256;
+      v[r] = rawP[i] + rawP[524288 + i];
+      s += v[r];
+      ss += v[r] * v[r];
+    }
+    breduce2(s, ss, red);
+    float mean = s * (1.f / 1024.f);
+    float var = ss * (1.f / 1024.f) - mean * mean;
+    float inv = rsqrtf(var + EPSN);
+#pragma unroll
+    for (int r = 0; r < 4; ++r) {
+      float t = (v[r] - mean) * inv;
+      t = t >= 0.f ? t : 0.2f * t;
+      Zt2[(size_t)(tid + r * 256) * 1024 + c] = f2bf(t);
+    }
+  }
+  gridbar(&bar[8]);
+
+  {
+    const int KF = 1024;
+    int wv = tid >> 6, lane = tid & 63;
+    int quad = lane >> 4, m16 = lane & 15;
+    int nb = (bid & 15) * 64, mb = ((bid >> 4) & 7) * 64, kh = bid >> 7;
+    const ushort* Ap = wfuse_bf + (size_t)(mb + wv * 16 + m16) * KF + kh * 512 + quad * 8;
+    const ushort* Bp = (const ushort*)Zt2 + (size_t)(nb + m16) * KF + kh * 512 + quad * 8;
+    f32x4 ac0 = {0.f, 0.f, 0.f, 0.f}, ac1 = ac0, ac2 = ac0, ac3 = ac0;
 #pragma unroll 4
-  for (int k0 = 0; k0 < 512; k0 += 32) {
-    bf16x8 af = *(const bf16x8*)(Ap + k0);
-    bf16x8 b0 = *(const bf16x8*)(Bp + k0);
-    bf16x8 b1 = *(const bf16x8*)(Bp + (size_t)16 * KF + k0);
-    bf16x8 b2 = *(const bf16x8*)(Bp + (size_t)32 * KF + k0);
-    bf16x8 b3 = *(const bf16x8*)(Bp + (size_t)48 * KF + k0);
-    ac0 = __builtin_amdgcn_mfma_f32_16x16x32_bf16(af, b0, ac0, 0, 0, 0);
-    ac1 = __builtin_amdgcn_mfma_f32_16x16x32_bf16(af, b1, ac1, 0, 0, 0);
-    ac2 = __builtin_amdgcn_mfma_f32_16x16x32_bf16(af, b2, ac2, 0, 0, 0);
-    ac3 = __builtin_amdgcn_mfma_f32_16x16x32_bf16(af, b3, ac3, 0, 0, 0);
-  }
-  int row = mb + wv * 16 + quad * 4;
-  float* C = Cp + (size_t)kh * 524288;
-  f32x4 accs[4] = {ac0, ac1, ac2, ac3};
-#pragma unroll
-  for (int nt = 0; nt < 4; ++nt)
-#pragma unroll
-    for (int r = 0; r < 4; ++r)
-      C[(size_t)(row + r) * N + nb + nt * 16 + m16] = accs[nt][r];
-}
-
-__global__ __launch_bounds__(256) void norm_down2(const float* __restrict__ ra,
-                                                  ushort* __restrict__ Zt2) {
-  __shared__ float red[8];
-  int c = blockIdx.x, tid = threadIdx.x;
-  float v[4];
-  float s = 0.f, ss = 0.f;
-#pragma unroll
-  for (int r = 0; r < 4; ++r) {
-    int i = c * 1024 + tid + r * 256;
-    v[r] = ra[i] + ra[524288 + i];
-    s += v[r];
-    ss += v[r] * v[r];
-  }
-  breduce2(s, ss, red);
-  float mean = s * (1.f / 1024.f);
-  float var = ss * (1.f / 1024.f) - mean * mean;
-  float inv = rsqrtf(var + EPSN);
-#pragma unroll
-  for (int r = 0; r < 4; ++r) {
-    float t = (v[r] - mean) * inv;
-    t = t >= 0.f ? t : 0.2f * t;
-    Zt2[(size_t)(tid + r * 256) * 1024 + c] = f2bf(t);
-  }
-}
-
-__global__ __launch_bounds__(256) void norm_leaky2(const float* __restrict__ ra,
-                                                   float* __restrict__ out) {
-  __shared__ float red[8];
-  int c = blockIdx.x, tid = threadIdx.x;
-  float v[4];
-  float s = 0.f, ss = 0.f;
-#pragma unroll
-  for (int r = 0; r < 4; ++r) {
-    int i = c * 1024 + tid + r * 256;
-    v[r] = ra[i] + ra[524288 + i];
-    s += v[r];
-    ss += v[r] * v[r];
-  }
-  breduce2(s, ss, red);
-  float mean = s * (1.f / 1024.f);
-  float var = ss * (1.f / 1024.f) - mean * mean;
-  float inv = rsqrtf(var + EPSN);
-#pragma unroll
-  for (int r = 0; r < 4; ++r) {
-    float t = (v[r] - mean) * inv;
-    out[c * 1024 + tid + r * 256] = t >= 0.f ? t : 0.2f * t;
+    for (int k0 = 0; k0 < 512; k0 += 32) {
+      bf16x8 af = *(const bf16x8*)(Ap + k0);
+      bf16x8 b0 = *(const bf16x8*)(Bp + k0);
+      bf16x8 b1 = *(const bf16x8*)(Bp + (size_t)16 * KF + k0);
+      bf16x8 b2 = *(const bf16x8*)(Bp + (size_t)32 * KF + k0);
+      bf16x8 b3 = *(const bf16x8*)(Bp + (size_t)48 * KF + k0);
+      ac0 = __builtin_amdgcn_mfma_f32_16x16x32_bf16(af, b0, ac0, 0, 0, 0);
+      ac1 = __builtin_amdgcn_mfma_f32_16x16x32_bf16(af, b1, ac1, 0, 0, 0);
+      ac2 = __builtin_amdgcn_mfma_f32_16x16x32_bf16(af, b2, ac2, 0, 0, 0);
+      ac3 = __builtin_amdgcn_mfma_f32_16x16x32_bf16(af, b3, ac3, 0, 0, 0);
+    }
+    int row = mb + wv * 16 + quad * 4;
+    float* C = rawP + (size_t)kh * 524288;
+    f32x4 accs[4] = {ac0, ac1, ac2, ac3};
+#pragma unroll
+    for (int nt = 0; nt < 4; ++nt)
+#pragma unroll
+      for (int r = 0; r < 4; ++r)
+        C[(size_t)(row + r) * 1024 + nb + nt * 16 + m16] = accs[nt][r];
+  }
+  gridbar(&bar[9]);
+
+  for (int vb = bid; vb < 512; vb += 256) {
+    int c = vb;
+    float v[4];
+    float s = 0.f, ss = 0.f;
+#pragma unroll
+    for (int r = 0; r < 4; ++r) {
+      int i = c * 1024 + tid + r * 256;
+      v[r] = rawP[i] + rawP[524288 + i];
+      s += v[r];
+      ss += v[r] * v[r];
+    }
+    breduce2(s, ss, red);
+    float mean = s * (1.f / 1024.f);
+    float var = ss * (1.f / 1024.f) - mean * mean;
+    float inv = rsqrtf(var + EPSN);
+#pragma unroll
+    for (int r = 0; r < 4; ++r) {
+      float t = (v[r] - mean) * inv;
+      out[c * 1024 + tid + r * 256] = t >= 0.f ? t : 0.2f * t;
+    }
   }
 }
 
@@ -685,9 +732,6 @@
   float* Zt2f = res + 524288;
   ushort* Zt2 = (ushort*)Zt2f;
   float* T = Zt2f + 524288;
-  ushort* feasRawH = (ushort*)T;
-  float* Apart = T;
-  ushort* Zt = (ushort*)T;
   float* orlt = T + 2097152;
   float* sigt = orlt + 524288;
   ushort* orlT = (ushort*)(sigt + 524288);
@@ -697,20 +741,13 @@
   ushort* resd = (ushort*)(sigt + 1867776);
   ushort* Apk_g = (ushort*)(sigt + 2916352);
   float* diagsum = sigt + 3268608;
+  unsigned* bar = (unsigned*)(diagsum + 256);
 
   pre_kernel<<<5569, 256, 0, stream>>>(gus, wdown, wfuse, w3, w5, w7, gus_bf,
                                        wdown_bf, wfuse_bf, resd, Apk_g, Acomb,
-                                       diagsum);
-  sk_mfma<<<256, 256, 0, stream>>>(x, Apk_g, feasRawH);
-  sk_norm<<<1536, 256, 0, stream>>>(feasRawH, feasH, bmean);
-  blend_fc<<<dim3(32, 16), 256, 0, stream>>>(feasH, bmean, wfc, bfc, w0, b0, w1,
-                                             b1, w2, b2, res, Zt2, resd);
-  gram_part2<<<dim3(10, 1, 32), 256, 0, stream>>>(res, Apart, diagsum);
-  attn_soft4<<<256, 256, 0, stream>>>(Apart, diagsum, Acomb);
-  tconv2<<<dim3(16, 16), 256, 0, stream>>>(Acomb, resd, orlt, sigt, orlT);
-  gus_csa<<<1152, 256, 0, stream>>>(gus_bf, orlT, sigt, orlt, Zt);
-  mfma_gemm_ks<<<dim3(16, 8, 2), 256, 0, stream>>>(wdown_bf, Zt, rawP, 1024);
-  norm_down2<<<512, 256, 0, stream>>>(rawP, Zt2);
-  mfma_gemm_ks<<<dim3(16, 8, 2), 256, 0, stream>>>(wfuse_bf, Zt2, rawP, 1024);
-  norm_leaky2<<<512, 256, 0, stream>>>(rawP, (float*)d_out);
-}
+                                       diagsum, bar);
+  mega<<<256, 256, 0, stream>>>(x, Apk_g, feasH, bmean, wfc, bfc, w0, b0, w1,
+                                b1, w2, b2, res, Zt2, resd, T, rawP, diagsum,
+                                orlt, sigt, orlT, gus_bf, wdown_bf, wfuse_bf,
+                                (float*)d_out, bar);
+}
```

New measurement: 448.2 us. 106% more time.
